# Kernel optimization log

Hardware: AMD Instinct MI355X
Metric: run time of the kernel (lower is better)

Reference implementation:

```python
import jax, jax.numpy as jnp
import numpy as np

_SAMPLING_EPS = 1e-5
_NEG_INF = -jnp.inf


def _apply_min_p(logits, min_p):
    # probs >= min_p * max_prob are kept (vLLM apply_min_p)
    probs = jax.nn.softmax(logits, axis=-1)
    max_p = jnp.max(probs, axis=-1, keepdims=True)
    keep = probs >= (min_p[:, None] * max_p)
    return jnp.where(keep, logits, _NEG_INF)


def _apply_top_k_top_p(logits, top_k, top_p):
    # One descending sort serves both filters (mirrors vLLM topk/topp kernel).
    T, V = logits.shape
    sorted_l = jnp.sort(logits, axis=-1)[:, ::-1]  # [T, V] descending
    # top-k threshold: k-th largest logit; top_k <= 0 means disabled
    k = jnp.where(top_k <= 0, V, jnp.clip(top_k, 1, V)).astype(jnp.int32)
    kth = jnp.take_along_axis(sorted_l, (k - 1)[:, None], axis=-1)  # [T, 1]
    # top-p: keep smallest prefix whose prob mass reaches top_p (first token always kept)
    probs = jax.nn.softmax(sorted_l, axis=-1)
    cum = jnp.cumsum(probs, axis=-1)
    keep_p = (cum - probs) < top_p[:, None]
    pth = jnp.min(jnp.where(keep_p, sorted_l, jnp.inf), axis=-1, keepdims=True)
    keep = (logits >= kth) & (logits >= pth)
    return jnp.where(keep, logits, _NEG_INF)


def _gather_logprobs(logprobs, num_logprobs, token_ids):
    # vLLM gather_logprobs: topk + sampled-token logprob + rank
    topk_lp, topk_idx = jax.lax.top_k(logprobs, num_logprobs)  # [T, K]
    tok = token_ids[:, None]  # [T, 1]
    tok_lp = jnp.take_along_axis(logprobs, tok, axis=-1)  # [T, 1]
    ranks = jnp.sum(logprobs >= tok_lp, axis=-1).astype(jnp.int32)  # [T]
    indices = jnp.concatenate([tok, topk_idx], axis=1).astype(jnp.int32)
    lps = jnp.concatenate([tok_lp, topk_lp], axis=1)
    return indices, lps, ranks


def setup_inputs() -> dict:
    key = jax.random.key(0)
    k1, k2, k3, k4, k5, k6 = jax.random.split(key, 6)
    T, V = 256, 128256
    logits = jax.random.normal(k1, (T, V), dtype=jnp.float32)
    temperature = 0.2 + 1.3 * jax.random.uniform(k2, (T,), dtype=jnp.float32)
    # every 8th request is greedy (temperature < _SAMPLING_EPS path)
    temperature = jnp.where(jnp.arange(T) % 8 == 0, 0.0, temperature)
    min_p = 0.05 * jax.random.uniform(k3, (T,), dtype=jnp.float32)
    top_p = 0.5 + 0.5 * jax.random.uniform(k4, (T,), dtype=jnp.float32)
    top_k = jax.random.randint(k5, (T,), 0, 64, dtype=jnp.int32)
    u = jax.random.uniform(k6, (T, V), dtype=jnp.float32, minval=1e-10, maxval=1.0)
    return {"logits": logits, "temperature": temperature, "min_p": min_p,
            "top_p": top_p, "top_k": top_k, "u": u, "num_logprobs": 20}


def reference(logits, temperature, min_p, top_p, top_k, u, num_logprobs):
    logits = logits.astype(jnp.float32)
    # logprobs computed on raw (pre-temperature) logits, as in vLLM
    raw_logprobs = jax.nn.log_softmax(logits, axis=-1)
    # greedy path
    greedy = jnp.argmax(logits, axis=-1)
    # random path: temperature -> min_p -> top-k/top-p -> gumbel-max sample
    is_greedy = temperature < _SAMPLING_EPS
    safe_temp = jnp.where(is_greedy, 1.0, temperature)  # rows with temp<eps use greedy anyway
    l = logits / safe_temp[:, None]
    l = _apply_min_p(l, min_p)
    l = _apply_top_k_top_p(l, top_k, top_p)
    gumbel = -jnp.log(-jnp.log(u))  # u in (0,1)
    random_sampled = jnp.argmax(l + gumbel, axis=-1)
    sampled = jnp.where(is_greedy, greedy, random_sampled)
    indices, lps, ranks = _gather_logprobs(raw_logprobs, num_logprobs, sampled)
    sampled_token_ids = sampled.astype(jnp.int32)[:, None]  # [T, 1]
    return sampled_token_ids, indices, lps, ranks
```

## Files before the change

### kernel.cpp

```cpp
#include <hip/hip_runtime.h>
#include <math.h>

#define TPB 1024
#define TPBS 256
#define NS 8
#define NBINS 512
#define CAP 2048
#define NSEL 64
#define MBINS 1024
#define MWIN 16.0f
#define WIN 2.0f
#define SLCAP 1024
#define BANDCAP 64

typedef unsigned long long u64t;

__device__ __forceinline__ unsigned int ordAsc(float v) {
  unsigned int b = __float_as_uint(v);
  return (b & 0x80000000u) ? ~b : (b | 0x80000000u);
}
__device__ __forceinline__ float ordInv(unsigned int o) {
  return __uint_as_float((o & 0x80000000u) ? (o & 0x7fffffffu) : ~o);
}
__device__ __forceinline__ unsigned int fkeyDesc(float v) { return ~ordAsc(v); }
__device__ __forceinline__ float fkeyInv(unsigned int kd) { return ordInv(~kd); }
__device__ __forceinline__ u64t mkMaxKey(float v, int idx) {
  return ((u64t)ordAsc(v) << 32) | (unsigned int)(~(unsigned int)idx);
}

__device__ __forceinline__ float blockSumF(float v, float* sred) {
  #pragma unroll
  for (int o = 32; o > 0; o >>= 1) v += __shfl_down(v, o, 64);
  int wid = threadIdx.x >> 6, lane = threadIdx.x & 63, nw = blockDim.x >> 6;
  __syncthreads();
  if (lane == 0) sred[wid] = v;
  __syncthreads();
  if (threadIdx.x == 0) { float r = sred[0]; for (int w = 1; w < nw; ++w) r += sred[w]; sred[0] = r; }
  __syncthreads();
  float r = sred[0];
  __syncthreads();
  return r;
}
__device__ __forceinline__ int blockSumI(int v, int* sred) {
  #pragma unroll
  for (int o = 32; o > 0; o >>= 1) v += __shfl_down(v, o, 64);
  int wid = threadIdx.x >> 6, lane = threadIdx.x & 63, nw = blockDim.x >> 6;
  __syncthreads();
  if (lane == 0) sred[wid] = v;
  __syncthreads();
  if (threadIdx.x == 0) { int r = sred[0]; for (int w = 1; w < nw; ++w) r += sred[w]; sred[0] = r; }
  __syncthreads();
  int r = sred[0];
  __syncthreads();
  return r;
}
__device__ __forceinline__ int blockMaxI(int v, int* sred) {
  #pragma unroll
  for (int o = 32; o > 0; o >>= 1) { int v2 = __shfl_down(v, o, 64); if (v2 > v) v = v2; }
  int wid = threadIdx.x >> 6, lane = threadIdx.x & 63, nw = blockDim.x >> 6;
  __syncthreads();
  if (lane == 0) sred[wid] = v;
  __syncthreads();
  if (threadIdx.x == 0) { int r = sred[0]; for (int w = 1; w < nw; ++w) if (sred[w] > r) r = sred[w]; sred[0] = r; }
  __syncthreads();
  int r = sred[0];
  __syncthreads();
  return r;
}
__device__ __forceinline__ u64t blockMaxU64(u64t v, u64t* sred) {
  #pragma unroll
  for (int o = 32; o > 0; o >>= 1) { u64t v2 = __shfl_down(v, o, 64); if (v2 > v) v = v2; }
  int wid = threadIdx.x >> 6, lane = threadIdx.x & 63, nw = blockDim.x >> 6;
  __syncthreads();
  if (lane == 0) sred[wid] = v;
  __syncthreads();
  if (threadIdx.x == 0) { u64t r = sred[0]; for (int w = 1; w < nw; ++w) if (sred[w] > r) r = sred[w]; sred[0] = r; }
  __syncthreads();
  u64t r = sred[0];
  __syncthreads();
  return r;
}
__device__ __forceinline__ void blockArgMaxF(float& v, int& idx, float* sredf, int* sredi) {
  #pragma unroll
  for (int o = 32; o > 0; o >>= 1) {
    float v2 = __shfl_down(v, o, 64);
    int  i2 = __shfl_down(idx, o, 64);
    if (v2 > v || (v2 == v && i2 < idx)) { v = v2; idx = i2; }
  }
  int wid = threadIdx.x >> 6, lane = threadIdx.x & 63, nw = blockDim.x >> 6;
  __syncthreads();
  if (lane == 0) { sredf[wid] = v; sredi[wid] = idx; }
  __syncthreads();
  if (threadIdx.x == 0) {
    float bv = sredf[0]; int bi = sredi[0];
    for (int w = 1; w < nw; ++w) {
      float v2 = sredf[w]; int i2 = sredi[w];
      if (v2 > bv || (v2 == bv && i2 < bi)) { bv = v2; bi = i2; }
    }
    sredf[0] = bv; sredi[0] = bi;
  }
  __syncthreads();
  v = sredf[0]; idx = sredi[0];
  __syncthreads();
}

__device__ void bitonicSortN(u64t* keys, int n) {
  for (unsigned int k = 2; k <= (unsigned int)n; k <<= 1) {
    for (unsigned int j = k >> 1; j > 0; j >>= 1) {
      __syncthreads();
      for (unsigned int i = threadIdx.x; i < (unsigned int)n; i += blockDim.x) {
        unsigned int ixj = i ^ j;
        if (ixj > i) {
          u64t a = keys[i], b = keys[ixj];
          bool up = ((i & k) == 0);
          if ((a > b) == up) { keys[i] = b; keys[ixj] = a; }
        }
      }
    }
  }
  __syncthreads();
}

__device__ u64t bitonicReg1024(u64t key, u64t* lds) {
  const int tid = threadIdx.x;
  for (unsigned int k = 2; k <= 1024; k <<= 1) {
    for (unsigned int j = k >> 1; j > 0; j >>= 1) {
      u64t partner;
      if (j >= 64) {
        __syncthreads();
        lds[tid] = key;
        __syncthreads();
        partner = lds[tid ^ j];
      } else {
        partner = __shfl_xor((unsigned long long)key, (int)j, 64);
      }
      bool up = ((tid & k) == 0);
      bool lower = ((tid & j) == 0);
      bool keepSmaller = (up == lower);
      bool pSmaller = (partner < key);
      if (keepSmaller == pSmaller) key = partner;
    }
  }
  __syncthreads();
  lds[tid] = key;
  __syncthreads();
  return key;
}

__device__ __forceinline__ float combineS0(const u64t* smax, const float* s0s, float m0) {
  float S0 = 0.f;
  for (int w = 0; w < NS; ++w) {
    float ms = ordInv((unsigned int)(smax[w] >> 32));
    S0 += s0s[w] * expf(ms - m0);
  }
  return S0;
}

__global__ __launch_bounds__(TPBS) void k1_max(const float* __restrict__ logits,
                                               u64t* __restrict__ maxes,
                                               float* __restrict__ s0_ws,
                                               int* __restrict__ ccnt,
                                               int* __restrict__ bandcnt, int V) {
  const int row = blockIdx.y, s = blockIdx.x, tid = threadIdx.x;
  if (s == 0 && tid == 0) { ccnt[row] = 0; bandcnt[row] = 0; }
  const float* x = logits + (size_t)row * V;
  const int V4 = V >> 2;
  const float4* x4 = (const float4*)x;
  const int a4 = (int)(((long long)V4 * s) / NS), b4 = (int)(((long long)V4 * (s + 1)) / NS);
  u64t best = 0ull;
  for (int i4 = a4 + tid; i4 < b4; i4 += TPBS) {
    float4 v = x4[i4]; int b = i4 << 2;
    u64t k0 = mkMaxKey(v.x, b);     if (k0 > best) best = k0;
    u64t k1 = mkMaxKey(v.y, b + 1); if (k1 > best) best = k1;
    u64t k2 = mkMaxKey(v.z, b + 2); if (k2 > best) best = k2;
    u64t k3 = mkMaxKey(v.w, b + 3); if (k3 > best) best = k3;
  }
  if (s == NS - 1) for (int i = (V4 << 2) + tid; i < V; i += TPBS) {
    u64t k = mkMaxKey(x[i], i); if (k > best) best = k;
  }
  __shared__ u64t sredU[16];
  __shared__ float sredF[16];
  best = blockMaxU64(best, sredU);
  if (tid == 0) maxes[row * NS + s] = best;
  const float msv = ordInv((unsigned int)(best >> 32));
  float s0 = 0.f;
  for (int i4 = a4 + tid; i4 < b4; i4 += TPBS) {
    float4 v = x4[i4];
    s0 += expf(v.x - msv) + expf(v.y - msv) + expf(v.z - msv) + expf(v.w - msv);
  }
  if (s == NS - 1) for (int i = (V4 << 2) + tid; i < V; i += TPBS) s0 += expf(x[i] - msv);
  float r0 = blockSumF(s0, sredF);
  if (tid == 0) s0_ws[row * NS + s] = r0;
}

__global__ __launch_bounds__(TPBS) void k2_all(const float* __restrict__ logits,
    const float* __restrict__ temp_arr, const float* __restrict__ minp_arr,
    const int* __restrict__ topk_arr, const u64t* __restrict__ maxes,
    float* __restrict__ sl_ws, float* __restrict__ sp_ws, int* __restrict__ ck_ws,
    int* __restrict__ ccnt, u64t* __restrict__ cand,
    int* __restrict__ bandcnt, u64t* __restrict__ band,
    u64t* __restrict__ mass, int V) {
  const int row = blockIdx.y, s = blockIdx.x, tid = threadIdx.x;
  __shared__ u64t smax[NS];
  __shared__ float sredF[16];
  __shared__ int sredI[16];
  __shared__ u64t lcand[SLCAP];
  __shared__ u64t lmass[MBINS];
  __shared__ int lcnt, lbase;
  const float temp = temp_arr[row];
  const bool greedy = (temp < 1e-5f);
  const int topk = topk_arr[row];
  const bool deep = (!greedy && topk <= 0);
  if (tid < NS) smax[tid] = maxes[row * NS + tid];
  if (tid == 0) lcnt = 0;
  if (deep) for (int b = tid; b < MBINS; b += TPBS) lmass[b] = 0ull;
  __syncthreads();
  u64t mk = smax[0];
  for (int w = 1; w < NS; ++w) { u64t t = smax[w]; if (t > mk) mk = t; }
  const float m0 = ordInv((unsigned int)(mk >> 32));
  const float wlo = m0 - WIN;
  const float* x = logits + (size_t)row * V;
  const int V4 = V >> 2;
  const float4* x4 = (const float4*)x;
  const int a4 = (int)(((long long)V4 * s) / NS), b4 = (int)(((long long)V4 * (s + 1)) / NS);

  if (greedy) {
    auto bodyG = [&](float vv, int gi) {
      if (vv >= wlo) {
        int pos = atomicAdd(&lcnt, 1);
        if (pos < SLCAP) lcand[pos] = ((u64t)fkeyDesc(vv) << 32) | (unsigned int)gi;
      }
    };
    for (int i4 = a4 + tid; i4 < b4; i4 += TPBS) {
      float4 v = x4[i4]; int b = i4 << 2;
      bodyG(v.x, b); bodyG(v.y, b + 1); bodyG(v.z, b + 2); bodyG(v.w, b + 3);
    }
    if (s == NS - 1) for (int i = (V4 << 2) + tid; i < V; i += TPBS) bodyG(x[i], i);
    __syncthreads();
    if (tid == 0) {
      sl_ws[row * NS + s] = 0.f; sp_ws[row * NS + s] = 0.f; ck_ws[row * NS + s] = 0;
      int c = lcnt;
      int add = (c > SLCAP) ? (c + CAP + 1) : c;
      lbase = atomicAdd(&ccnt[row], add);
    }
    __syncthreads();
    int c = lcnt < SLCAP ? lcnt : SLCAP;
    int base = lbase;
    for (int j = tid; j < c; j += TPBS) {
      int pos = base + j;
      if (pos < CAP) cand[(size_t)row * CAP + pos] = lcand[j];
    }
    return;
  }

  const float st = temp;
  const float ml = m0 / st;
  const float minp = minp_arr[row];
  const float bHi = minp * (1.0f + 4e-6f);
  const float bLo = minp * (1.0f - 4e-6f);
  const float scaleM = (float)MBINS / MWIN;
  float sl = 0.f, sp = 0.f; int ckp = 0;
  auto body = [&](float vv, int gi) {
    float l = vv / st;
    float e = expf(l - ml);
    sl += e;
    if (minp <= 0.f || e > bHi) {
      sp += e; ckp++;
      if (deep) {
        float fm = (m0 - vv) * scaleM;
        if (fm < (float)MBINS)
          atomicAdd(&lmass[(int)fm], (u64t)((double)e * 4294967296.0));
      }
    } else if (e >= bLo) {
      int pos = atomicAdd(&bandcnt[row], 1);
      if (pos < BANDCAP)
        band[(size_t)row * BANDCAP + pos] = ((u64t)(unsigned int)gi << 32) | __float_as_uint(vv);
    }
    if (vv >= wlo) {
      int pos = atomicAdd(&lcnt, 1);
      if (pos < SLCAP) lcand[pos] = ((u64t)fkeyDesc(vv) << 32) | (unsigned int)gi;
    }
  };
  for (int i4 = a4 + tid; i4 < b4; i4 += TPBS) {
    float4 v = x4[i4]; int b = i4 << 2;
    body(v.x, b); body(v.y, b + 1); body(v.z, b + 2); body(v.w, b + 3);
  }
  if (s == NS - 1) for (int i = (V4 << 2) + tid; i < V; i += TPBS) body(x[i], i);
  float rl = blockSumF(sl, sredF);
  float rp = blockSumF(sp, sredF);
  int rc = blockSumI(ckp, sredI);
  if (tid == 0) {
    sl_ws[row * NS + s] = rl; sp_ws[row * NS + s] = rp; ck_ws[row * NS + s] = rc;
    int c = lcnt;
    int add = (c > SLCAP) ? (c + CAP + 1) : c;
    lbase = atomicAdd(&ccnt[row], add);
  }
  __syncthreads();
  int c = lcnt < SLCAP ? lcnt : SLCAP;
  int base = lbase;
  for (int j = tid; j < c; j += TPBS) {
    int pos = base + j;
    if (pos < CAP) cand[(size_t)row * CAP + pos] = lcand[j];
  }
  if (deep) {
    u64t* mrow = mass + ((size_t)row * NS + s) * MBINS;
    for (int b = tid; b < MBINS; b += TPBS) mrow[b] = lmass[b];
  }
}

__global__ __launch_bounds__(TPB) void k5_final(const float* __restrict__ logits,
    const float* __restrict__ temp_arr, const float* __restrict__ minp_arr,
    const float* __restrict__ topp_arr, const int* __restrict__ topk_arr,
    const float* __restrict__ u_arr, const u64t* __restrict__ maxes,
    const float* __restrict__ s0_ws, const float* __restrict__ sl_ws,
    const float* __restrict__ sp_ws, const int* __restrict__ ck_ws,
    const int* __restrict__ ccnt, const u64t* __restrict__ cand,
    const u64t* __restrict__ mass, const u64t* __restrict__ band,
    const int* __restrict__ bandcnt, float* __restrict__ w_thr,
    int* __restrict__ w_bpM, double* __restrict__ w_seed, float* __restrict__ w_spD,
    float* __restrict__ out, int T, int V, int NL) {
  __shared__ u64t keyA[CAP];
  __shared__ int fh[NBINS];
  __shared__ float sredF[16];
  __shared__ int sredI[16];
  __shared__ u64t smax[NS];
  __shared__ float sp0[NS], spl[NS], spsp[NS];
  __shared__ int spck[NS];
  __shared__ float sh_thresh, sh_toklp, sh_spAdd;
  __shared__ double sh_seed;
  __shared__ int sh_cnt, sh_bp, sh_bCnt, sh_ckAdd;
  __shared__ u64t sh_bKeys[BANDCAP];
  __shared__ u64t sh_bMass[BANDCAP];
  __shared__ int  sh_bBin[BANDCAP];
  __shared__ u64t kb64[NSEL];
  __shared__ u64t kbs[NSEL];

  const int row = blockIdx.x;
  const int tid = threadIdx.x;
  const float* x  = logits + (size_t)row * V;
  const float* uu = u_arr  + (size_t)row * V;
  const float temp = temp_arr[row];
  const float minp = minp_arr[row];
  const float topp = topp_arr[row];
  const int   topk = topk_arr[row];
  const bool greedy = (temp < 1e-5f);
  const float st = greedy ? 1.0f : temp;
  const int V4 = V >> 2;
  const float4* x4 = (const float4*)x;

  if (tid < NS) {
    smax[tid] = maxes[row * NS + tid];
    sp0[tid] = s0_ws[row * NS + tid];
    spl[tid] = sl_ws[row * NS + tid];
    spsp[tid] = sp_ws[row * NS + tid];
    spck[tid] = ck_ws[row * NS + tid];
  }
  __syncthreads();
  u64t mk = smax[0];
  for (int w = 1; w < NS; ++w) { u64t t = smax[w]; if (t > mk) mk = t; }
  const float m0 = ordInv((unsigned int)(mk >> 32));
  const int gidx = (int)(~(unsigned int)mk);
  float S = spl[0], Sp = spsp[0];
  int ck = spck[0];
  for (int w = 1; w < NS; ++w) { S += spl[w]; Sp += spsp[w]; ck += spck[w]; }
  const float S0 = combineS0(smax, sp0, m0);
  const float ml = m0 / st;
  const float logS0 = logf(S0);
  const float rhs = minp * (1.0f / S);
  const float rhsS = rhs * S;
  const float rhsHi = rhsS * (1.0f + 1e-6f);
  const float rhsLo = rhsS * (1.0f - 1e-6f);
  auto keepTest = [&](float e) -> bool {
    if (e > rhsHi) return true;
    if (e < rhsLo) return false;
    return (e / S) >= rhs;
  };
  const bool deep = (!greedy && topk <= 0);
  const float scaleM = (float)MBINS / MWIN;

  const int bandTotal = greedy ? 0 : bandcnt[row];
  const bool bandOv = bandTotal > BANDCAP;
  if (tid == 0) { sh_bCnt = 0; sh_spAdd = 0.f; sh_ckAdd = 0; }
  __syncthreads();
  if (!greedy && !bandOv && bandTotal > 0 && minp > 0.f) {
    if (tid == 0) {
      for (int i = 0; i < bandTotal; ++i) sh_bKeys[i] = band[(size_t)row * BANDCAP + i];
      for (int i = 1; i < bandTotal; ++i) {
        u64t k = sh_bKeys[i]; int j = i - 1;
        while (j >= 0 && sh_bKeys[j] > k) { sh_bKeys[j + 1] = sh_bKeys[j]; j--; }
        sh_bKeys[j + 1] = k;
      }
      float spAdd = 0.f; int ckAdd = 0, bc = 0;
      for (int i = 0; i < bandTotal; ++i) {
        float vv = __uint_as_float((unsigned int)(sh_bKeys[i] & 0xffffffffu));
        float l = vv / st; float e = expf(l - ml);
        if ((e / S) >= rhs) {
          spAdd += e; ckAdd++;
          if (deep) {
            float fm = (m0 - vv) * scaleM;
            if (fm < (float)MBINS) { sh_bBin[bc] = (int)fm; sh_bMass[bc] = (u64t)((double)e * 4294967296.0); bc++; }
          }
        }
      }
      sh_spAdd = spAdd; sh_ckAdd = ckAdd; sh_bCnt = bc;
    }
    __syncthreads();
    Sp += sh_spAdd; ck += sh_ckAdd;
  } else if (!greedy && bandOv) {
    float sp2 = 0.f; int ck2 = 0;
    auto bodyR = [&](float vv) {
      float l = vv / st; float e = expf(l - ml);
      if (keepTest(e)) { sp2 += e; ck2++; }
    };
    for (int i4 = tid; i4 < V4; i4 += TPB) { float4 v = x4[i4]; bodyR(v.x); bodyR(v.y); bodyR(v.z); bodyR(v.w); }
    for (int i = (V4 << 2) + tid; i < V; i += TPB) bodyR(x[i]);
    Sp = blockSumF(sp2, sredF);
    ck = blockSumI(ck2, sredI);
  }

  int cc = ccnt[row];
  int Cact = cc < CAP ? cc : CAP;
  int need = NSEL;
  if (topk > need) need = topk;
  if (need > CAP / 2) need = CAP / 2;
  if (need > V) need = V;
  bool fb = (cc > CAP) || (Cact < need);
  if (!fb) {
    for (int j = tid; j < Cact; j += TPB) keyA[j] = cand[(size_t)row * CAP + j];
  } else {
    const float bS = (float)NBINS / MWIN;
    for (int b = tid; b < NBINS; b += TPB) fh[b] = 0;
    if (tid == 0) sh_cnt = 0;
    __syncthreads();
    auto hb = [&](float vv) {
      float fbv = (m0 - vv) * bS;
      if (fbv < (float)NBINS) atomicAdd(&fh[(int)fbv], 1);
    };
    for (int i4 = tid; i4 < V4; i4 += TPB) { float4 v = x4[i4]; hb(v.x); hb(v.y); hb(v.z); hb(v.w); }
    for (int i = (V4 << 2) + tid; i < V; i += TPB) hb(x[i]);
    __syncthreads();
    if (tid == 0) {
      int cum = 0, B = -1;
      for (int b = 0; b < NBINS; ++b) { cum += fh[b]; if (cum >= need) { B = b; break; } }
      if (B < 0) B = NBINS - 1;
      sh_bp = B;
    }
    __syncthreads();
    const int B = sh_bp;
    auto cb = [&](float vv, int gi) {
      float fbv = (m0 - vv) * bS;
      if (fbv < (float)NBINS && (int)fbv <= B) {
        int pos = atomicAdd(&sh_cnt, 1);
        if (pos < CAP) keyA[pos] = ((u64t)fkeyDesc(vv) << 32) | (unsigned int)gi;
      }
    };
    for (int i4 = tid; i4 < V4; i4 += TPB) { float4 v = x4[i4]; int b = i4 << 2; cb(v.x, b); cb(v.y, b + 1); cb(v.z, b + 2); cb(v.w, b + 3); }
    for (int i = (V4 << 2) + tid; i < V; i += TPB) cb(x[i], i);
    __syncthreads();
    Cact = sh_cnt < CAP ? sh_cnt : CAP;
  }
  __syncthreads();
  if (Cact <= 1024) {
    u64t ka = (tid < Cact) ? keyA[tid] : ~0ull;
    bitonicReg1024(ka, keyA);
  } else {
    int n = 128; while (n < Cact) n <<= 1;
    for (int i = Cact + tid; i < n; i += TPB) keyA[i] = ~0ull;
    __syncthreads();
    bitonicSortN(keyA, n);
  }
  {
    int M = Cact < NSEL ? Cact : NSEL;
    if (tid < M) {
      u64t ka = keyA[tid];
      float xv = fkeyInv((unsigned int)(ka >> 32));
      float lp = (xv - m0) - logS0;
      kb64[tid] = ((u64t)fkeyDesc(lp) << 32) | (ka & 0xffffffffu);
    }
    __syncthreads();
    if (tid < M) {
      u64t me = kb64[tid];
      int r = 0;
      for (int i = 0; i < M; ++i) r += (kb64[i] < me) ? 1 : 0;
      kbs[r] = me;
    }
    __syncthreads();
    float* o_idx  = out + T;
    float* o_lps  = out + T + (size_t)T * (NL + 1);
    for (int j = tid; j < NL; j += TPB) {
      if (j < M) {
        u64t kb = kbs[j];
        o_idx[(size_t)row * (NL + 1) + 1 + j] = (float)(unsigned int)(kb & 0xffffffffu);
        o_lps[(size_t)row * (NL + 1) + 1 + j] = fkeyInv((unsigned int)(kb >> 32));
      }
    }
  }

  int sampled = -1;
  if (greedy) {
    sampled = gidx;
  } else if (topk > 0) {
    if (tid == 0) {
      int k = topk; if (k > V) k = V; if (k > CAP) k = CAP;
      int jp = 0; float cum = 0.f;
      for (int j = 0; j < k; ++j) {
        float pj = 0.f;
        if (j < ck && j < Cact) {
          float xv = fkeyInv((unsigned int)(keyA[j] >> 32));
          pj = expf(xv / st - ml) / Sp;
        }
        cum += pj;
        float ex = cum - pj;
        if (ex < topp) jp = j;
      }
      float thr;
      if (jp < ck && jp < Cact) {
        float xv = fkeyInv((unsigned int)(keyA[jp] >> 32));
        thr = xv / st;
      } else thr = -INFINITY;
      sh_thresh = thr;
    }
    __syncthreads();
    const float thr = sh_thresh;
    float bm = -INFINITY; int bi = 0x7fffffff;
    for (int j = tid; j < Cact; j += TPB) {
      u64t ka = keyA[j];
      float xv = fkeyInv((unsigned int)(ka >> 32));
      int gi = (int)(ka & 0xffffffffu);
      float l = xv / st;
      float e = expf(l - ml);
      if (keepTest(e) && l >= thr) {
        float uv = uu[gi];
        float g = -logf(-logf(uv));
        float val = l + g;
        if (val > bm || (val == bm && gi < bi)) { bm = val; bi = gi; }
      }
    }
    blockArgMaxF(bm, bi, sredF, sredI);
    sampled = bi;
  } else {
    if (!bandOv) {
      if (tid < MBINS) {
        u64t m = 0;
        for (int w = 0; w < NS; ++w) m += mass[((size_t)row * NS + w) * MBINS + tid];
        int bc = sh_bCnt;
        for (int j = 0; j < bc; ++j) if (sh_bBin[j] == tid) m += sh_bMass[j];
        keyA[tid] = m;
      }
    } else {
      for (int b = tid; b < MBINS; b += TPB) keyA[b] = 0ull;
      __syncthreads();
      auto bodyM = [&](float vv) {
        float l = vv / st; float e = expf(l - ml);
        if (keepTest(e)) {
          float fm = (m0 - vv) * scaleM;
          if (fm < (float)MBINS) atomicAdd(&keyA[(int)fm], (u64t)((double)e * 4294967296.0));
        }
      };
      for (int i4 = tid; i4 < V4; i4 += TPB) { float4 v = x4[i4]; bodyM(v.x); bodyM(v.y); bodyM(v.z); bodyM(v.w); }
      for (int i = (V4 << 2) + tid; i < V; i += TPB) bodyM(x[i]);
    }
    __syncthreads();
    u64t mh = (tid < MBINS) ? keyA[tid] : 0ull;
    for (int off = 1; off < MBINS; off <<= 1) {
      u64t add = (tid < MBINS && tid >= off) ? keyA[tid - off] : 0ull;
      __syncthreads();
      if (tid < MBINS) keyA[tid] += add;
      __syncthreads();
    }
    const double TP = (double)topp * (double)Sp;
    int q = -1; u64t myexcl = 0;
    if (tid < MBINS && mh > 0ull) {
      u64t excl = keyA[tid] - mh;
      if ((double)excl * (1.0 / 4294967296.0) < TP) { q = tid; myexcl = excl; }
    }
    int bp = blockMaxI(q, sredI);
    if (bp >= 0 && tid == bp) sh_seed = (double)myexcl * (1.0 / 4294967296.0);
    if (bp < 0 && tid == 0) sh_seed = 0.0;
    __syncthreads();
    if (tid == 0) {
      w_bpM[row] = bp;
      w_seed[row] = sh_seed;
      w_spD[row] = Sp;
      if (bp < 0) w_thr[row] = -INFINITY;
    }
  }

  if (!deep) {
    if (tid == 0) sh_toklp = (x[sampled] - m0) - logS0;
    __syncthreads();
    const float toklp = sh_toklp;
    int rc = 0;
    for (int j = tid; j < Cact; j += TPB) {
      float xv = fkeyInv((unsigned int)(keyA[j] >> 32));
      float lp = (xv - m0) - logS0;
      if (lp >= toklp) rc++;
    }
    int rank = blockSumI(rc, sredI);
    float* o_samp = out;
    float* o_idx  = out + T;
    float* o_lps  = out + T + (size_t)T * (NL + 1);
    float* o_rank = out + T + (size_t)2 * T * (NL + 1);
    if (tid == 0) {
      o_samp[row] = (float)sampled;
      o_idx[(size_t)row * (NL + 1)] = (float)sampled;
      o_lps[(size_t)row * (NL + 1)] = toklp;
      o_rank[row] = (float)rank;
    }
  }
}

__global__ __launch_bounds__(TPB) void kD_thr(const float* __restrict__ logits,
    const float* __restrict__ temp_arr, const float* __restrict__ minp_arr,
    const float* __restrict__ topp_arr, const int* __restrict__ topk_arr,
    const u64t* __restrict__ maxes, const float* __restrict__ sl_ws,
    const int* __restrict__ w_bpM, const float* __restrict__ w_spD,
    const double* __restrict__ w_seed, float* __restrict__ w_thr, int V) {
  const int row = blockIdx.x, tid = threadIdx.x;
  const float temp = temp_arr[row];
  if (temp < 1e-5f || topk_arr[row] > 0) return;
  const int bp = w_bpM[row];
  if (bp < 0) return;
  __shared__ u64t keyA[CAP];
  __shared__ float pvals[CAP];
  __shared__ u64t smax[NS];
  __shared__ float ssl[NS];
  __shared__ int sh_cnt;
  if (tid < NS) { smax[tid] = maxes[row * NS + tid]; ssl[tid] = sl_ws[row * NS + tid]; }
  if (tid == 0) sh_cnt = 0;
  __syncthreads();
  u64t mk = smax[0];
  for (int w = 1; w < NS; ++w) { u64t t = smax[w]; if (t > mk) mk = t; }
  float S = ssl[0];
  for (int w = 1; w < NS; ++w) S += ssl[w];
  const float m0 = ordInv((unsigned int)(mk >> 32));
  const float st = temp;
  const float ml = m0 / st;
  const float minp = minp_arr[row];
  const float rhs = minp * (1.0f / S);
  const float rhsS = rhs * S;
  const float rhsHi = rhsS * (1.0f + 1e-6f);
  const float rhsLo = rhsS * (1.0f - 1e-6f);
  auto keepTest = [&](float e) -> bool {
    if (e > rhsHi) return true;
    if (e < rhsLo) return false;
    return (e / S) >= rhs;
  };
  const float scaleM = (float)MBINS / MWIN;
  const float* x = logits + (size_t)row * V;
  const int V4 = V >> 2;
  const float4* x4 = (const float4*)x;
  auto body = [&](float vv, int gi) {
    float fm = (m0 - vv) * scaleM;
    if (fm < (float)MBINS && (int)fm == bp) {
      float l = vv / st;
      float e = expf(l - ml);
      if (keepTest(e)) {
        int pos = atomicAdd(&sh_cnt, 1);
        if (pos < CAP) keyA[pos] = ((u64t)fkeyDesc(vv) << 32) | (unsigned int)gi;
      }
    }
  };
  for (int i4 = tid; i4 < V4; i4 += TPB) {
    float4 v = x4[i4]; int b = i4 << 2;
    body(v.x, b); body(v.y, b + 1); body(v.z, b + 2); body(v.w, b + 3);
  }
  for (int i = (V4 << 2) + tid; i < V; i += TPB) body(x[i], i);
  __syncthreads();
  int C5 = sh_cnt < CAP ? sh_cnt : CAP;
  if (C5 <= 1024) {
    u64t kc = (tid < C5) ? keyA[tid] : ~0ull;
    bitonicReg1024(kc, keyA);
  } else {
    int n5 = 128; while (n5 < C5) n5 <<= 1;
    for (int i = C5 + tid; i < n5; i += TPB) keyA[i] = ~0ull;
    __syncthreads();
    bitonicSortN(keyA, n5);
  }
  const float Sp = w_spD[row];
  for (int j = tid; j < C5; j += TPB) {
    float xv = fkeyInv((unsigned int)(keyA[j] >> 32));
    pvals[j] = expf(xv / st - ml) / Sp;
  }
  __syncthreads();
  if (tid == 0) {
    const float topp = topp_arr[row];
    float cum = (float)(w_seed[row] / (double)Sp);
    float lastVal = fkeyInv((unsigned int)(keyA[0] >> 32));
    for (int j = 0; j < C5; ++j) {
      float pj = pvals[j];
      cum += pj;
      float ex = cum - pj;
      if (ex < topp) lastVal = fkeyInv((unsigned int)(keyA[j] >> 32));
    }
    w_thr[row] = lastVal / st;
  }
}

__global__ __launch_bounds__(TPBS) void k6_gumbel(const float* __restrict__ logits,
    const float* __restrict__ temp_arr, const float* __restrict__ minp_arr,
    const int* __restrict__ topk_arr, const float* __restrict__ u_arr,
    const u64t* __restrict__ maxes, const float* __restrict__ sl_ws,
    const float* __restrict__ w_thr, u64t* __restrict__ gkey, int V) {
  const int row = blockIdx.y, s = blockIdx.x, tid = threadIdx.x;
  const float temp = temp_arr[row];
  if (temp < 1e-5f || topk_arr[row] > 0) return;
  __shared__ u64t smax[NS];
  __shared__ float ssl[NS];
  __shared__ float sredF[16];
  __shared__ int sredI[16];
  if (tid < NS) { smax[tid] = maxes[row * NS + tid]; ssl[tid] = sl_ws[row * NS + tid]; }
  __syncthreads();
  u64t mk = smax[0];
  for (int w = 1; w < NS; ++w) { u64t t = smax[w]; if (t > mk) mk = t; }
  float S = ssl[0];
  for (int w = 1; w < NS; ++w) S += ssl[w];
  const float m0 = ordInv((unsigned int)(mk >> 32));
  const float st = temp;
  const float ml = m0 / st;
  const float minp = minp_arr[row];
  const float rhs = minp * (1.0f / S);
  const float rhsS = rhs * S;
  const float rhsHi = rhsS * (1.0f + 1e-6f);
  const float rhsLo = rhsS * (1.0f - 1e-6f);
  auto keepTest = [&](float e) -> bool {
    if (e > rhsHi) return true;
    if (e < rhsLo) return false;
    return (e / S) >= rhs;
  };
  const float thr = w_thr[row];
  const float* x  = logits + (size_t)row * V;
  const float* uu = u_arr  + (size_t)row * V;
  const int V4 = V >> 2;
  const float4* x4 = (const float4*)x;
  const float4* u4 = (const float4*)uu;
  const int a4 = (int)(((long long)V4 * s) / NS), b4 = (int)(((long long)V4 * (s + 1)) / NS);
  float bm = -INFINITY; int bi = 0x7fffffff;
  auto body = [&](float vv, float uv, int gi) {
    float l = vv / st;
    float e = expf(l - ml);
    if (keepTest(e) && l >= thr) {
      float g = -logf(-logf(uv));
      float val = l + g;
      if (val > bm || (val == bm && gi < bi)) { bm = val; bi = gi; }
    }
  };
  for (int i4 = a4 + tid; i4 < b4; i4 += TPBS) {
    float4 v = x4[i4]; float4 w = u4[i4]; int b = i4 << 2;
    body(v.x, w.x, b); body(v.y, w.y, b + 1); body(v.z, w.z, b + 2); body(v.w, w.w, b + 3);
  }
  if (s == NS - 1) for (int i = (V4 << 2) + tid; i < V; i += TPBS) body(x[i], uu[i], i);
  blockArgMaxF(bm, bi, sredF, sredI);
  if (tid == 0) gkey[row * NS + s] = mkMaxKey(bm, bi);
}

__global__ __launch_bounds__(TPB) void k7_deepfin(const float* __restrict__ logits,
    const float* __restrict__ temp_arr, const int* __restrict__ topk_arr,
    const u64t* __restrict__ gkey, const float* __restrict__ s0_ws,
    const u64t* __restrict__ maxes, float* __restrict__ out, int T, int V, int NL) {
  const int row = blockIdx.x, tid = threadIdx.x;
  const float temp = temp_arr[row];
  if (temp < 1e-5f || topk_arr[row] > 0) return;
  __shared__ u64t sg[NS];
  __shared__ u64t smax[NS];
  __shared__ float sp0[NS];
  __shared__ int sredI[16];
  if (tid < NS) { sg[tid] = gkey[row * NS + tid]; smax[tid] = maxes[row * NS + tid]; sp0[tid] = s0_ws[row * NS + tid]; }
  __syncthreads();
  u64t gk = sg[0];
  for (int w = 1; w < NS; ++w) { if (sg[w] > gk) gk = sg[w]; }
  u64t mk = smax[0];
  for (int w = 1; w < NS; ++w) { u64t t = smax[w]; if (t > mk) mk = t; }
  const float m0 = ordInv((unsigned int)(mk >> 32));
  const float S0 = combineS0(smax, sp0, m0);
  const float logS0 = logf(S0);
  const int sampled = (int)(~(unsigned int)gk);
  const float* x = logits + (size_t)row * V;
  const float toklp = (x[sampled] - m0) - logS0;
  const int V4 = V >> 2;
  const float4* x4 = (const float4*)x;
  int rc = 0;
  auto body = [&](float vv) {
    float lp = (vv - m0) - logS0;
    if (lp >= toklp) rc++;
  };
  for (int i4 = tid; i4 < V4; i4 += TPB) { float4 v = x4[i4]; body(v.x); body(v.y); body(v.z); body(v.w); }
  for (int i = (V4 << 2) + tid; i < V; i += TPB) body(x[i]);
  int rank = blockSumI(rc, sredI);
  float* o_samp = out;
  float* o_idx  = out + T;
  float* o_lps  = out + T + (size_t)T * (NL + 1);
  float* o_rank = out + T + (size_t)2 * T * (NL + 1);
  if (tid == 0) {
    o_samp[row] = (float)sampled;
    o_idx[(size_t)row * (NL + 1)] = (float)sampled;
    o_lps[(size_t)row * (NL + 1)] = toklp;
    o_rank[row] = (float)rank;
  }
}

__global__ __launch_bounds__(TPB) void sampler_mono(
    const float* __restrict__ logits, const float* __restrict__ temp_arr,
    const float* __restrict__ minp_arr, const float* __restrict__ topp_arr,
    const int* __restrict__ topk_arr, const float* __restrict__ u_arr,
    float* __restrict__ out, int T, int V, int NL) {
  __shared__ u64t keyA[CAP];
  __shared__ u64t keyB[CAP];
  __shared__ float pvals[CAP];
  __shared__ int   cnthist[NBINS];
  __shared__ u64t  masshist[NBINS];
  __shared__ float sredF[16];
  __shared__ int   sredI[16];
  __shared__ float sh_thresh, sh_toklp, sh_Rm, sh_Roff;
  __shared__ double sh_seedD, sh_seedBase;
  __shared__ int sh_B64, sh_Bp, sh_cnt, sh_state;

  const int row = blockIdx.x;
  const int tid = threadIdx.x;
  const float* x  = logits + (size_t)row * V;
  const float* uu = u_arr  + (size_t)row * V;
  const float temp = temp_arr[row];
  const float minp = minp_arr[row];
  const float topp = topp_arr[row];
  const int   topk = topk_arr[row];
  const bool greedy = (temp < 1e-5f);
  const float st = greedy ? 1.0f : temp;
  const int V4 = V >> 2;
  const float4* x4 = (const float4*)x;

  float m0; int gidx;
  {
    float lm = -INFINITY; int lidx = 0x7fffffff;
    for (int i4 = tid; i4 < V4; i4 += TPB) {
      float4 v = x4[i4]; int b = i4 << 2;
      if (v.x > lm) { lm = v.x; lidx = b; }
      if (v.y > lm) { lm = v.y; lidx = b + 1; }
      if (v.z > lm) { lm = v.z; lidx = b + 2; }
      if (v.w > lm) { lm = v.w; lidx = b + 3; }
    }
    for (int i = (V4 << 2) + tid; i < V; i += TPB) {
      float v = x[i]; if (v > lm) { lm = v; lidx = i; }
    }
    blockArgMaxF(lm, lidx, sredF, sredI);
    m0 = lm; gidx = lidx;
  }
  const float ml = m0 / st;

  float Rcur = 2.0f;
  float binScale = (float)NBINS / Rcur;
  for (int b = tid; b < NBINS; b += TPB) cnthist[b] = 0;
  __syncthreads();
  float S0, S;
  {
    float s0p = 0.f, slp = 0.f;
    auto histAdd = [&](float vv) {
      float fb = (m0 - vv) * binScale;
      if (fb < (float)NBINS) atomicAdd(&cnthist[(int)fb], 1);
    };
    for (int i4 = tid; i4 < V4; i4 += TPB) {
      float4 v = x4[i4];
      s0p += expf(v.x - m0) + expf(v.y - m0) + expf(v.z - m0) + expf(v.w - m0);
      if (!greedy) slp += expf(v.x / st - ml) + expf(v.y / st - ml) + expf(v.z / st - ml) + expf(v.w / st - ml);
      histAdd(v.x); histAdd(v.y); histAdd(v.z); histAdd(v.w);
    }
    for (int i = (V4 << 2) + tid; i < V; i += TPB) {
      float v = x[i]; s0p += expf(v - m0); if (!greedy) slp += expf(v / st - ml); histAdd(v);
    }
    S0 = blockSumF(s0p, sredF);
    S = greedy ? S0 : blockSumF(slp, sredF);
  }

  int need = NSEL;
  if (topk > need) need = topk;
  if (need > CAP / 2) need = CAP / 2;
  if (need > V) need = V;
  int B64;
  for (int attempt = 0; ; ++attempt) {
    __syncthreads();
    if (tid == 0) {
      long long cum = 0; int b64 = -1; long long c64 = 0;
      for (int b = 0; b < NBINS; ++b) {
        cum += cnthist[b];
        if (cum >= need) { b64 = b; c64 = cum; break; }
      }
      int state;
      if (b64 >= 0 && c64 <= CAP) state = 1;
      else if (b64 < 0) state = 0;
      else state = 2;
      if (attempt >= 3 && state != 1) { state = 1; if (b64 < 0) b64 = NBINS - 1; }
      sh_state = state; sh_B64 = b64;
    }
    __syncthreads();
    if (sh_state == 1) { B64 = sh_B64; break; }
    Rcur = (sh_state == 0) ? Rcur * 8.0f : Rcur * 0.125f;
    binScale = (float)NBINS / Rcur;
    __syncthreads();
    for (int b = tid; b < NBINS; b += TPB) cnthist[b] = 0;
    __syncthreads();
    auto histAdd2 = [&](float vv) {
      float fb = (m0 - vv) * binScale;
      if (fb < (float)NBINS) atomicAdd(&cnthist[(int)fb], 1);
    };
    for (int i4 = tid; i4 < V4; i4 += TPB) {
      float4 v = x4[i4];
      histAdd2(v.x); histAdd2(v.y); histAdd2(v.z); histAdd2(v.w);
    }
    for (int i = (V4 << 2) + tid; i < V; i += TPB) histAdd2(x[i]);
  }

  const float logS0 = logf(S0);
  const float rhs = minp * (1.0f / S);
  const float rhsS = rhs * S;
  const float rhsHi = rhsS * (1.0f + 1e-6f);
  const float rhsLo = rhsS * (1.0f - 1e-6f);
  auto keepTest = [&](float e) -> bool {
    if (e > rhsHi) return true;
    if (e < rhsLo) return false;
    return (e / S) >= rhs;
  };
  const bool needMass = (!greedy && topk <= 0);
  const float scaleM0 = (float)NBINS / 16.0f;

  for (int b = tid; b < NBINS; b += TPB) { cnthist[b] = 0; masshist[b] = 0ull; }
  if (tid == 0) { sh_cnt = 0; sh_Rm = 16.0f; sh_Roff = 0.0f; sh_seedBase = 0.0; }
  __syncthreads();
  float Sp; int ck;
  {
    float spp = 0.f; int ckp = 0;
    auto bodyB = [&](float vv, int gi) {
      float fb = (m0 - vv) * binScale;
      if (fb < (float)NBINS && (int)fb <= B64) {
        int pos = atomicAdd(&sh_cnt, 1);
        if (pos < CAP) keyA[pos] = ((u64t)fkeyDesc(vv) << 32) | (unsigned int)gi;
      }
      if (!greedy) {
        float l = vv / st;
        float e = expf(l - ml);
        if (keepTest(e)) {
          spp += e; ckp++;
          if (needMass) {
            float fm = (m0 - vv) * scaleM0;
            if (fm < (float)NBINS) {
              int bm = (int)fm;
              atomicAdd(&masshist[bm], (u64t)((double)e * 4294967296.0));
              atomicAdd(&cnthist[bm], 1);
            }
          }
        }
      }
    };
    for (int i4 = tid; i4 < V4; i4 += TPB) {
      float4 v = x4[i4]; int b = i4 << 2;
      bodyB(v.x, b); bodyB(v.y, b + 1); bodyB(v.z, b + 2); bodyB(v.w, b + 3);
    }
    for (int i = (V4 << 2) + tid; i < V; i += TPB) bodyB(x[i], i);
    Sp = blockSumF(spp, sredF);
    ck = blockSumI(ckp, sredI);
  }
  int Cact = sh_cnt; if (Cact > CAP) Cact = CAP;

  int n = 128; while (n < Cact) n <<= 1;
  for (int i = Cact + tid; i < n; i += TPB) keyA[i] = ~0ull;
  __syncthreads();
  bitonicSortN(keyA, n);
  for (int j = tid; j < n; j += TPB) {
    if (j < Cact) {
      u64t ka = keyA[j];
      float xv = fkeyInv((unsigned int)(ka >> 32));
      float lp = (xv - m0) - logS0;
      keyB[j] = ((u64t)fkeyDesc(lp) << 32) | (ka & 0xffffffffu);
    } else keyB[j] = ~0ull;
  }
  bitonicSortN(keyB, n);

  int sampled;
  if (greedy) {
    sampled = gidx;
  } else if (topk > 0) {
    if (tid == 0) {
      int k = topk; if (k > V) k = V; if (k > CAP) k = CAP;
      int jp = 0; float cum = 0.f;
      for (int j = 0; j < k; ++j) {
        float pj = 0.f;
        if (j < ck && j < Cact) {
          float xv = fkeyInv((unsigned int)(keyA[j] >> 32));
          pj = expf(xv / st - ml) / Sp;
        }
        cum += pj;
        float ex = cum - pj;
        if (ex < topp) jp = j;
      }
      float thr;
      if (jp < ck && jp < Cact) {
        float xv = fkeyInv((unsigned int)(keyA[jp] >> 32));
        thr = xv / st;
      } else thr = -INFINITY;
      sh_thresh = thr;
    }
    __syncthreads();
    const float thr = sh_thresh;
    float bm = -INFINITY; int bi = 0x7fffffff;
    for (int j = tid; j < Cact; j += TPB) {
      u64t ka = keyA[j];
      float xv = fkeyInv((unsigned int)(ka >> 32));
      int gi = (int)(ka & 0xffffffffu);
      float l = xv / st;
      float e = expf(l - ml);
      if (keepTest(e) && l >= thr) {
        float uv = uu[gi];
        float g = -logf(-logf(uv));
        float val = l + g;
        if (val > bm || (val == bm && gi < bi)) { bm = val; bi = gi; }
      }
    }
    blockArgMaxF(bm, bi, sredF, sredI);
    sampled = bi;
  } else {
    for (int attempt = 0; ; ++attempt) {
      __syncthreads();
      if (tid == 0) {
        float Rm = sh_Rm, Roff = sh_Roff;
        double TP = (double)topp * (double)Sp;
        double cm = sh_seedBase; int bp = -1; double seed = sh_seedBase; int cbp = 0;
        for (int b = 0; b < NBINS; ++b) {
          u64t mh = masshist[b];
          if (mh > 0ull && cm < TP) { bp = b; seed = cm; cbp = cnthist[b]; }
          cm += (double)mh * (1.0 / 4294967296.0);
        }
        int state = 1;
        if (attempt < 3) {
          if (cm < TP && Roff == 0.0f) {
            state = 0; sh_Rm = Rm * 8.0f;
          } else if (bp >= 0 && cbp > CAP) {
            state = 2;
            float bw = Rm / (float)NBINS;
            sh_Roff = Roff + (float)bp * bw;
            sh_Rm = bw;
            sh_seedBase = seed;
          }
        }
        if (bp < 0) { bp = 0; seed = sh_seedBase; }
        sh_Bp = bp; sh_seedD = seed; sh_state = state;
      }
      __syncthreads();
      if (sh_state == 1) break;
      float Rm = sh_Rm, Roff = sh_Roff;
      float sM = (float)NBINS / Rm;
      for (int b = tid; b < NBINS; b += TPB) { cnthist[b] = 0; masshist[b] = 0ull; }
      __syncthreads();
      auto bodyM = [&](float vv) {
        float fm = ((m0 - vv) - Roff) * sM;
        if (fm >= 0.f && fm < (float)NBINS) {
          float l = vv / st;
          float e = expf(l - ml);
          if (keepTest(e)) {
            int bm = (int)fm;
            atomicAdd(&masshist[bm], (u64t)((double)e * 4294967296.0));
            atomicAdd(&cnthist[bm], 1);
          }
        }
      };
      for (int i4 = tid; i4 < V4; i4 += TPB) {
        float4 v = x4[i4]; bodyM(v.x); bodyM(v.y); bodyM(v.z); bodyM(v.w);
      }
      for (int i = (V4 << 2) + tid; i < V; i += TPB) bodyM(x[i]);
    }
    const int Bp = sh_Bp;
    const float RmF = sh_Rm, RoffF = sh_Roff;
    const float sM = (float)NBINS / RmF;
    if (tid == 0) sh_cnt = 0;
    __syncthreads();
    auto bodyC = [&](float vv, int gi) {
      float fm = ((m0 - vv) - RoffF) * sM;
      if (fm >= 0.f && fm < (float)NBINS && (int)fm == Bp) {
        float l = vv / st;
        float e = expf(l - ml);
        if (keepTest(e)) {
          int pos = atomicAdd(&sh_cnt, 1);
          if (pos < CAP) keyA[pos] = ((u64t)fkeyDesc(vv) << 32) | (unsigned int)gi;
        }
      }
    };
    for (int i4 = tid; i4 < V4; i4 += TPB) {
      float4 v = x4[i4]; int b = i4 << 2;
      bodyC(v.x, b); bodyC(v.y, b + 1); bodyC(v.z, b + 2); bodyC(v.w, b + 3);
    }
    for (int i = (V4 << 2) + tid; i < V; i += TPB) bodyC(x[i], i);
    __syncthreads();
    int C5 = sh_cnt; if (C5 > CAP) C5 = CAP;
    int n5 = 128; while (n5 < C5) n5 <<= 1;
    for (int i = C5 + tid; i < n5; i += TPB) keyA[i] = ~0ull;
    __syncthreads();
    bitonicSortN(keyA, n5);
    for (int j = tid; j < C5; j += TPB) {
      float xv = fkeyInv((unsigned int)(keyA[j] >> 32));
      pvals[j] = expf(xv / st - ml) / Sp;
    }
    __syncthreads();
    if (tid == 0) {
      float cum = (float)(sh_seedD / (double)Sp);
      float lastVal = fkeyInv((unsigned int)(keyA[0] >> 32));
      for (int j = 0; j < C5; ++j) {
        float pj = pvals[j];
        cum += pj;
        float ex = cum - pj;
        if (ex < topp) lastVal = fkeyInv((unsigned int)(keyA[j] >> 32));
      }
      sh_thresh = lastVal / st;
    }
    __syncthreads();
    const float thr = sh_thresh;
    const float4* u4 = (const float4*)uu;
    float bm = -INFINITY; int bi = 0x7fffffff;
    auto body6 = [&](float vv, float uv, int gi) {
      float l = vv / st;
      float e = expf(l - ml);
      if (keepTest(e) && l >= thr) {
        float g = -logf(-logf(uv));
        float val = l + g;
        if (val > bm || (val == bm && gi < bi)) { bm = val; bi = gi; }
      }
    };
    for (int i4 = tid; i4 < V4; i4 += TPB) {
      float4 v = x4[i4]; float4 w = u4[i4]; int b = i4 << 2;
      body6(v.x, w.x, b); body6(v.y, w.y, b + 1); body6(v.z, w.z, b + 2); body6(v.w, w.w, b + 3);
    }
    for (int i = (V4 << 2) + tid; i < V; i += TPB) body6(x[i], uu[i], i);
    blockArgMaxF(bm, bi, sredF, sredI);
    sampled = bi;
  }

  if (tid == 0) sh_toklp = (x[sampled] - m0) - logS0;
  __syncthreads();
  const float toklp = sh_toklp;
  int rank;
  {
    int rc = 0;
    if (!needMass) {
      for (int j = tid; j < Cact; j += TPB) {
        float xv = fkeyInv((unsigned int)(keyA[j] >> 32));
        float lp = (xv - m0) - logS0;
        if (lp >= toklp) rc++;
      }
    } else {
      auto body7 = [&](float vv) {
        float lp = (vv - m0) - logS0;
        if (lp >= toklp) rc++;
      };
      for (int i4 = tid; i4 < V4; i4 += TPB) {
        float4 v = x4[i4]; body7(v.x); body7(v.y); body7(v.z); body7(v.w);
      }
      for (int i = (V4 << 2) + tid; i < V; i += TPB) body7(x[i]);
    }
    rank = blockSumI(rc, sredI);
  }

  float* o_samp = out;
  float* o_idx  = out + T;
  float* o_lps  = out + T + (size_t)T * (NL + 1);
  float* o_rank = out + T + (size_t)2 * T * (NL + 1);
  if (tid == 0) {
    o_samp[row] = (float)sampled;
    o_idx[(size_t)row * (NL + 1)] = (float)sampled;
    o_lps[(size_t)row * (NL + 1)] = toklp;
    o_rank[row] = (float)rank;
  }
  for (int j = tid; j < NL; j += TPB) {
    u64t kb = keyB[j];
    o_idx[(size_t)row * (NL + 1) + 1 + j] = (float)(unsigned int)(kb & 0xffffffffu);
    o_lps[(size_t)row * (NL + 1) + 1 + j] = fkeyInv((unsigned int)(kb >> 32));
  }
}

extern "C" void kernel_launch(void* const* d_in, const int* in_sizes, int n_in,
                              void* d_out, int out_size, void* d_ws, size_t ws_size,
                              hipStream_t stream) {
  const float* logits = (const float*)d_in[0];
  const float* temp   = (const float*)d_in[1];
  const float* minp   = (const float*)d_in[2];
  const float* topp   = (const float*)d_in[3];
  const int*   topk   = (const int*)d_in[4];
  const float* u      = (const float*)d_in[5];
  const int T  = in_sizes[1];
  const int V  = in_sizes[0] / T;
  const int NL = (out_size / T - 4) / 2;

  size_t off = 0;
  char* base = (char*)d_ws;
  u64t*   w_maxes   = (u64t*)(base + off);   off += (size_t)T * NS * 8;
  u64t*   w_cand    = (u64t*)(base + off);   off += (size_t)T * CAP * 8;
  u64t*   w_mass    = (u64t*)(base + off);   off += (size_t)T * NS * MBINS * 8;
  u64t*   w_gkey    = (u64t*)(base + off);   off += (size_t)T * NS * 8;
  u64t*   w_band    = (u64t*)(base + off);   off += (size_t)T * BANDCAP * 8;
  double* w_seed    = (double*)(base + off); off += (size_t)T * 8;
  float*  w_s0      = (float*)(base + off);  off += (size_t)T * NS * 4;
  float*  w_sl      = (float*)(base + off);  off += (size_t)T * NS * 4;
  float*  w_sp      = (float*)(base + off);  off += (size_t)T * NS * 4;
  int*    w_ck      = (int*)(base + off);    off += (size_t)T * NS * 4;
  int*    w_ccnt    = (int*)(base + off);    off += (size_t)T * 4;
  int*    w_bandcnt = (int*)(base + off);    off += (size_t)T * 4;
  float*  w_thr     = (float*)(base + off);  off += (size_t)T * 4;
  int*    w_bpM     = (int*)(base + off);    off += (size_t)T * 4;
  float*  w_spD     = (float*)(base + off);  off += (size_t)T * 4;

  if (off > ws_size) {
    sampler_mono<<<T, TPB, 0, stream>>>(logits, temp, minp, topp, topk, u,
                                        (float*)d_out, T, V, NL);
    return;
  }

  dim3 gS(NS, T);
  k1_max<<<gS, TPBS, 0, stream>>>(logits, w_maxes, w_s0, w_ccnt, w_bandcnt, V);
  k2_all<<<gS, TPBS, 0, stream>>>(logits, temp, minp, topk, w_maxes, w_sl,
                                  w_sp, w_ck, w_ccnt, w_cand, w_bandcnt, w_band,
                                  w_mass, V);
  k5_final<<<T, TPB, 0, stream>>>(logits, temp, minp, topp, topk, u, w_maxes,
                                  w_s0, w_sl, w_sp, w_ck, w_ccnt, w_cand, w_mass,
                                  w_band, w_bandcnt, w_thr, w_bpM, w_seed, w_spD,
                                  (float*)d_out, T, V, NL);
  kD_thr<<<T, TPB, 0, stream>>>(logits, temp, minp, topp, topk, w_maxes, w_sl,
                                w_bpM, w_spD, w_seed, w_thr, V);
  k6_gumbel<<<gS, TPBS, 0, stream>>>(logits, temp, minp, topk, u, w_maxes, w_sl,
                                     w_thr, w_gkey, V);
  k7_deepfin<<<T, TPB, 0, stream>>>(logits, temp, topk, w_gkey, w_s0, w_maxes,
                                    (float*)d_out, T, V, NL);
}
```

Baseline: 212.7 us.

## Fuse sampler pipeline into one kernel with per-row inter-block spin barriers

Replaces the six-kernel chain (max, stats, final, threshold, gumbel, deep-finish) with a single fused kernel plus a small zeroing kernel. Each row is now handled by 4 cooperating blocks instead of 8, and they synchronise through global atomic counters used as row-level barriers. The separate exp-sum pass from the old max kernel is folded into the stats pass using the global row max. This targets launch gaps and repeated reads of the logits. The cost is that the grid relies on all blocks of a row being resident at once for the spin barriers to finish, and each row now gets less parallelism.

```diff
diff --git a/kernel.cpp b/kernel.cpp
--- a/kernel.cpp
+++ b/kernel.cpp
@@ -1,10 +1,12 @@
 #include <hip/hip_runtime.h>
 #include <math.h>
 
+#define TPBS 256
 #define TPB 1024
-#define TPBS 256
-#define NS 8
+#define NS 4
+#define NBAR 8
 #define NBINS 512
+#define FBBINS 256
 #define CAP 2048
 #define NSEL 64
 #define MBINS 1024
@@ -121,222 +123,52 @@
   __syncthreads();
 }
 
-__device__ u64t bitonicReg1024(u64t key, u64t* lds) {
-  const int tid = threadIdx.x;
-  for (unsigned int k = 2; k <= 1024; k <<= 1) {
-    for (unsigned int j = k >> 1; j > 0; j >>= 1) {
-      u64t partner;
-      if (j >= 64) {
-        __syncthreads();
-        lds[tid] = key;
-        __syncthreads();
-        partner = lds[tid ^ j];
-      } else {
-        partner = __shfl_xor((unsigned long long)key, (int)j, 64);
-      }
-      bool up = ((tid & k) == 0);
-      bool lower = ((tid & j) == 0);
-      bool keepSmaller = (up == lower);
-      bool pSmaller = (partner < key);
-      if (keepSmaller == pSmaller) key = partner;
-    }
-  }
-  __syncthreads();
-  lds[tid] = key;
-  __syncthreads();
-  return key;
-}
-
-__device__ __forceinline__ float combineS0(const u64t* smax, const float* s0s, float m0) {
-  float S0 = 0.f;
-  for (int w = 0; w < NS; ++w) {
-    float ms = ordInv((unsigned int)(smax[w] >> 32));
-    S0 += s0s[w] * expf(ms - m0);
-  }
-  return S0;
-}
-
-__global__ __launch_bounds__(TPBS) void k1_max(const float* __restrict__ logits,
-                                               u64t* __restrict__ maxes,
-                                               float* __restrict__ s0_ws,
-                                               int* __restrict__ ccnt,
-                                               int* __restrict__ bandcnt, int V) {
-  const int row = blockIdx.y, s = blockIdx.x, tid = threadIdx.x;
-  if (s == 0 && tid == 0) { ccnt[row] = 0; bandcnt[row] = 0; }
-  const float* x = logits + (size_t)row * V;
-  const int V4 = V >> 2;
-  const float4* x4 = (const float4*)x;
-  const int a4 = (int)(((long long)V4 * s) / NS), b4 = (int)(((long long)V4 * (s + 1)) / NS);
-  u64t best = 0ull;
-  for (int i4 = a4 + tid; i4 < b4; i4 += TPBS) {
-    float4 v = x4[i4]; int b = i4 << 2;
-    u64t k0 = mkMaxKey(v.x, b);     if (k0 > best) best = k0;
-    u64t k1 = mkMaxKey(v.y, b + 1); if (k1 > best) best = k1;
-    u64t k2 = mkMaxKey(v.z, b + 2); if (k2 > best) best = k2;
-    u64t k3 = mkMaxKey(v.w, b + 3); if (k3 > best) best = k3;
-  }
-  if (s == NS - 1) for (int i = (V4 << 2) + tid; i < V; i += TPBS) {
-    u64t k = mkMaxKey(x[i], i); if (k > best) best = k;
-  }
-  __shared__ u64t sredU[16];
-  __shared__ float sredF[16];
-  best = blockMaxU64(best, sredU);
-  if (tid == 0) maxes[row * NS + s] = best;
-  const float msv = ordInv((unsigned int)(best >> 32));
-  float s0 = 0.f;
-  for (int i4 = a4 + tid; i4 < b4; i4 += TPBS) {
-    float4 v = x4[i4];
-    s0 += expf(v.x - msv) + expf(v.y - msv) + expf(v.z - msv) + expf(v.w - msv);
-  }
-  if (s == NS - 1) for (int i = (V4 << 2) + tid; i < V; i += TPBS) s0 += expf(x[i] - msv);
-  float r0 = blockSumF(s0, sredF);
-  if (tid == 0) s0_ws[row * NS + s] = r0;
-}
-
-__global__ __launch_bounds__(TPBS) void k2_all(const float* __restrict__ logits,
-    const float* __restrict__ temp_arr, const float* __restrict__ minp_arr,
-    const int* __restrict__ topk_arr, const u64t* __restrict__ maxes,
-    float* __restrict__ sl_ws, float* __restrict__ sp_ws, int* __restrict__ ck_ws,
-    int* __restrict__ ccnt, u64t* __restrict__ cand,
-    int* __restrict__ bandcnt, u64t* __restrict__ band,
-    u64t* __restrict__ mass, int V) {
-  const int row = blockIdx.y, s = blockIdx.x, tid = threadIdx.x;
+__device__ __forceinline__ void rowBarrier(int* ctr) {
+  __syncthreads();
+  __threadfence();
+  if (threadIdx.x == 0) {
+    atomicAdd(ctr, 1);
+    while (__hip_atomic_load(ctr, __ATOMIC_ACQUIRE, __HIP_MEMORY_SCOPE_AGENT) < NS)
+      __builtin_amdgcn_s_sleep(2);
+  }
+  __syncthreads();
+  __threadfence();
+}
+
+__global__ void k0_zero(int* __restrict__ p, int n) {
+  int i = blockIdx.x * blockDim.x + threadIdx.x;
+  if (i < n) p[i] = 0;
+}
+
+__global__ __launch_bounds__(TPBS, 6) void fused(
+    const float* __restrict__ logits, const float* __restrict__ temp_arr,
+    const float* __restrict__ minp_arr, const float* __restrict__ topp_arr,
+    const int* __restrict__ topk_arr, const float* __restrict__ u_arr,
+    u64t* __restrict__ maxes, u64t* __restrict__ cand, u64t* __restrict__ mass,
+    u64t* __restrict__ gkey, u64t* __restrict__ band,
+    float* __restrict__ s0_ws, float* __restrict__ sl_ws, float* __restrict__ sp_ws,
+    int* __restrict__ ck_ws, int* __restrict__ ccnt, int* __restrict__ bandcnt,
+    int* __restrict__ ccnt2, int* __restrict__ rankAcc,
+    float* __restrict__ w_thr, int* __restrict__ w_bp,
+    int* __restrict__ w_sampled, float* __restrict__ w_toklp,
+    int* __restrict__ bars, float* __restrict__ out, int T, int V, int NL) {
+  __shared__ u64t bufA[CAP];
   __shared__ u64t smax[NS];
+  __shared__ float s0s[NS], sls[NS], sps[NS];
+  __shared__ int scks[NS];
   __shared__ float sredF[16];
   __shared__ int sredI[16];
-  __shared__ u64t lcand[SLCAP];
-  __shared__ u64t lmass[MBINS];
-  __shared__ int lcnt, lbase;
-  const float temp = temp_arr[row];
-  const bool greedy = (temp < 1e-5f);
-  const int topk = topk_arr[row];
-  const bool deep = (!greedy && topk <= 0);
-  if (tid < NS) smax[tid] = maxes[row * NS + tid];
-  if (tid == 0) lcnt = 0;
-  if (deep) for (int b = tid; b < MBINS; b += TPBS) lmass[b] = 0ull;
-  __syncthreads();
-  u64t mk = smax[0];
-  for (int w = 1; w < NS; ++w) { u64t t = smax[w]; if (t > mk) mk = t; }
-  const float m0 = ordInv((unsigned int)(mk >> 32));
-  const float wlo = m0 - WIN;
-  const float* x = logits + (size_t)row * V;
-  const int V4 = V >> 2;
-  const float4* x4 = (const float4*)x;
-  const int a4 = (int)(((long long)V4 * s) / NS), b4 = (int)(((long long)V4 * (s + 1)) / NS);
-
-  if (greedy) {
-    auto bodyG = [&](float vv, int gi) {
-      if (vv >= wlo) {
-        int pos = atomicAdd(&lcnt, 1);
-        if (pos < SLCAP) lcand[pos] = ((u64t)fkeyDesc(vv) << 32) | (unsigned int)gi;
-      }
-    };
-    for (int i4 = a4 + tid; i4 < b4; i4 += TPBS) {
-      float4 v = x4[i4]; int b = i4 << 2;
-      bodyG(v.x, b); bodyG(v.y, b + 1); bodyG(v.z, b + 2); bodyG(v.w, b + 3);
-    }
-    if (s == NS - 1) for (int i = (V4 << 2) + tid; i < V; i += TPBS) bodyG(x[i], i);
-    __syncthreads();
-    if (tid == 0) {
-      sl_ws[row * NS + s] = 0.f; sp_ws[row * NS + s] = 0.f; ck_ws[row * NS + s] = 0;
-      int c = lcnt;
-      int add = (c > SLCAP) ? (c + CAP + 1) : c;
-      lbase = atomicAdd(&ccnt[row], add);
-    }
-    __syncthreads();
-    int c = lcnt < SLCAP ? lcnt : SLCAP;
-    int base = lbase;
-    for (int j = tid; j < c; j += TPBS) {
-      int pos = base + j;
-      if (pos < CAP) cand[(size_t)row * CAP + pos] = lcand[j];
-    }
-    return;
-  }
-
-  const float st = temp;
-  const float ml = m0 / st;
-  const float minp = minp_arr[row];
-  const float bHi = minp * (1.0f + 4e-6f);
-  const float bLo = minp * (1.0f - 4e-6f);
-  const float scaleM = (float)MBINS / MWIN;
-  float sl = 0.f, sp = 0.f; int ckp = 0;
-  auto body = [&](float vv, int gi) {
-    float l = vv / st;
-    float e = expf(l - ml);
-    sl += e;
-    if (minp <= 0.f || e > bHi) {
-      sp += e; ckp++;
-      if (deep) {
-        float fm = (m0 - vv) * scaleM;
-        if (fm < (float)MBINS)
-          atomicAdd(&lmass[(int)fm], (u64t)((double)e * 4294967296.0));
-      }
-    } else if (e >= bLo) {
-      int pos = atomicAdd(&bandcnt[row], 1);
-      if (pos < BANDCAP)
-        band[(size_t)row * BANDCAP + pos] = ((u64t)(unsigned int)gi << 32) | __float_as_uint(vv);
-    }
-    if (vv >= wlo) {
-      int pos = atomicAdd(&lcnt, 1);
-      if (pos < SLCAP) lcand[pos] = ((u64t)fkeyDesc(vv) << 32) | (unsigned int)gi;
-    }
-  };
-  for (int i4 = a4 + tid; i4 < b4; i4 += TPBS) {
-    float4 v = x4[i4]; int b = i4 << 2;
-    body(v.x, b); body(v.y, b + 1); body(v.z, b + 2); body(v.w, b + 3);
-  }
-  if (s == NS - 1) for (int i = (V4 << 2) + tid; i < V; i += TPBS) body(x[i], i);
-  float rl = blockSumF(sl, sredF);
-  float rp = blockSumF(sp, sredF);
-  int rc = blockSumI(ckp, sredI);
-  if (tid == 0) {
-    sl_ws[row * NS + s] = rl; sp_ws[row * NS + s] = rp; ck_ws[row * NS + s] = rc;
-    int c = lcnt;
-    int add = (c > SLCAP) ? (c + CAP + 1) : c;
-    lbase = atomicAdd(&ccnt[row], add);
-  }
-  __syncthreads();
-  int c = lcnt < SLCAP ? lcnt : SLCAP;
-  int base = lbase;
-  for (int j = tid; j < c; j += TPBS) {
-    int pos = base + j;
-    if (pos < CAP) cand[(size_t)row * CAP + pos] = lcand[j];
-  }
-  if (deep) {
-    u64t* mrow = mass + ((size_t)row * NS + s) * MBINS;
-    for (int b = tid; b < MBINS; b += TPBS) mrow[b] = lmass[b];
-  }
-}
-
-__global__ __launch_bounds__(TPB) void k5_final(const float* __restrict__ logits,
-    const float* __restrict__ temp_arr, const float* __restrict__ minp_arr,
-    const float* __restrict__ topp_arr, const int* __restrict__ topk_arr,
-    const float* __restrict__ u_arr, const u64t* __restrict__ maxes,
-    const float* __restrict__ s0_ws, const float* __restrict__ sl_ws,
-    const float* __restrict__ sp_ws, const int* __restrict__ ck_ws,
-    const int* __restrict__ ccnt, const u64t* __restrict__ cand,
-    const u64t* __restrict__ mass, const u64t* __restrict__ band,
-    const int* __restrict__ bandcnt, float* __restrict__ w_thr,
-    int* __restrict__ w_bpM, double* __restrict__ w_seed, float* __restrict__ w_spD,
-    float* __restrict__ out, int T, int V, int NL) {
-  __shared__ u64t keyA[CAP];
-  __shared__ int fh[NBINS];
-  __shared__ float sredF[16];
-  __shared__ int sredI[16];
-  __shared__ u64t smax[NS];
-  __shared__ float sp0[NS], spl[NS], spsp[NS];
-  __shared__ int spck[NS];
-  __shared__ float sh_thresh, sh_toklp, sh_spAdd;
-  __shared__ double sh_seed;
-  __shared__ int sh_cnt, sh_bp, sh_bCnt, sh_ckAdd;
+  __shared__ u64t sredU[16];
   __shared__ u64t sh_bKeys[BANDCAP];
   __shared__ u64t sh_bMass[BANDCAP];
   __shared__ int  sh_bBin[BANDCAP];
-  __shared__ u64t kb64[NSEL];
-  __shared__ u64t kbs[NSEL];
-
-  const int row = blockIdx.x;
-  const int tid = threadIdx.x;
+  __shared__ u64t kbuf[2 * NSEL];
+  __shared__ int lcnt, lbase, sh_cnt, sh_bCnt, sh_ckAdd;
+  __shared__ float sh_thresh, sh_spAdd;
+  __shared__ double sh_seedD;
+
+  const int s = blockIdx.x, row = blockIdx.y, tid = threadIdx.x;
+  int* myBar = bars + row * NBAR;
   const float* x  = logits + (size_t)row * V;
   const float* uu = u_arr  + (size_t)row * V;
   const float temp = temp_arr[row];
@@ -344,458 +176,522 @@
   const float topp = topp_arr[row];
   const int   topk = topk_arr[row];
   const bool greedy = (temp < 1e-5f);
+  const bool deep = (!greedy && topk <= 0);
   const float st = greedy ? 1.0f : temp;
   const int V4 = V >> 2;
   const float4* x4 = (const float4*)x;
-
-  if (tid < NS) {
-    smax[tid] = maxes[row * NS + tid];
-    sp0[tid] = s0_ws[row * NS + tid];
-    spl[tid] = sl_ws[row * NS + tid];
-    spsp[tid] = sp_ws[row * NS + tid];
-    spck[tid] = ck_ws[row * NS + tid];
-  }
+  const int a4 = (int)(((long long)V4 * s) / NS), b4 = (int)(((long long)V4 * (s + 1)) / NS);
+
+  {
+    u64t best = 0ull;
+    for (int i4 = a4 + tid; i4 < b4; i4 += TPBS) {
+      float4 v = x4[i4]; int b = i4 << 2;
+      u64t k0 = mkMaxKey(v.x, b);     if (k0 > best) best = k0;
+      u64t k1 = mkMaxKey(v.y, b + 1); if (k1 > best) best = k1;
+      u64t k2 = mkMaxKey(v.z, b + 2); if (k2 > best) best = k2;
+      u64t k3 = mkMaxKey(v.w, b + 3); if (k3 > best) best = k3;
+    }
+    if (s == NS - 1) for (int i = (V4 << 2) + tid; i < V; i += TPBS) {
+      u64t k = mkMaxKey(x[i], i); if (k > best) best = k;
+    }
+    best = blockMaxU64(best, sredU);
+    if (tid == 0) maxes[row * NS + s] = best;
+  }
+  rowBarrier(&myBar[0]);
+
+  if (tid < NS) smax[tid] = maxes[row * NS + tid];
+  if (tid == 0) lcnt = 0;
   __syncthreads();
   u64t mk = smax[0];
   for (int w = 1; w < NS; ++w) { u64t t = smax[w]; if (t > mk) mk = t; }
   const float m0 = ordInv((unsigned int)(mk >> 32));
   const int gidx = (int)(~(unsigned int)mk);
-  float S = spl[0], Sp = spsp[0];
-  int ck = spck[0];
-  for (int w = 1; w < NS; ++w) { S += spl[w]; Sp += spsp[w]; ck += spck[w]; }
-  const float S0 = combineS0(smax, sp0, m0);
   const float ml = m0 / st;
-  const float logS0 = logf(S0);
+  const float wlo = m0 - WIN;
+  const float bHi = minp * (1.0f + 4e-6f);
+  const float bLo = minp * (1.0f - 4e-6f);
+  const float scaleM = (float)MBINS / MWIN;
+  {
+    u64t* lcand = bufA;
+    u64t* lmass = bufA + SLCAP;
+    if (deep) for (int b = tid; b < MBINS; b += TPBS) lmass[b] = 0ull;
+    __syncthreads();
+    float s0 = 0.f, sl = 0.f, sp = 0.f; int ckp = 0;
+    if (greedy) {
+      auto bodyG = [&](float vv, int gi) {
+        s0 += expf(vv - m0);
+        if (vv >= wlo) {
+          int pos = atomicAdd(&lcnt, 1);
+          if (pos < SLCAP) lcand[pos] = ((u64t)fkeyDesc(vv) << 32) | (unsigned int)gi;
+        }
+      };
+      for (int i4 = a4 + tid; i4 < b4; i4 += TPBS) {
+        float4 v = x4[i4]; int b = i4 << 2;
+        bodyG(v.x, b); bodyG(v.y, b + 1); bodyG(v.z, b + 2); bodyG(v.w, b + 3);
+      }
+      if (s == NS - 1) for (int i = (V4 << 2) + tid; i < V; i += TPBS) bodyG(x[i], i);
+    } else {
+      auto body = [&](float vv, int gi) {
+        s0 += expf(vv - m0);
+        float l = vv / st;
+        float e = expf(l - ml);
+        sl += e;
+        if (minp <= 0.f || e > bHi) {
+          sp += e; ckp++;
+          if (deep) {
+            float fm = (m0 - vv) * scaleM;
+            if (fm < (float)MBINS)
+              atomicAdd(&lmass[(int)fm], (u64t)((double)e * 4294967296.0));
+          }
+        } else if (e >= bLo) {
+          int pos = atomicAdd(&bandcnt[row], 1);
+          if (pos < BANDCAP)
+            band[(size_t)row * BANDCAP + pos] = ((u64t)(unsigned int)gi << 32) | __float_as_uint(vv);
+        }
+        if (vv >= wlo) {
+          int pos = atomicAdd(&lcnt, 1);
+          if (pos < SLCAP) lcand[pos] = ((u64t)fkeyDesc(vv) << 32) | (unsigned int)gi;
+        }
+      };
+      for (int i4 = a4 + tid; i4 < b4; i4 += TPBS) {
+        float4 v = x4[i4]; int b = i4 << 2;
+        body(v.x, b); body(v.y, b + 1); body(v.z, b + 2); body(v.w, b + 3);
+      }
+      if (s == NS - 1) for (int i = (V4 << 2) + tid; i < V; i += TPBS) body(x[i], i);
+    }
+    float r0 = blockSumF(s0, sredF);
+    float rl = blockSumF(sl, sredF);
+    float rp = blockSumF(sp, sredF);
+    int rc = blockSumI(ckp, sredI);
+    if (tid == 0) {
+      s0_ws[row * NS + s] = r0; sl_ws[row * NS + s] = rl;
+      sp_ws[row * NS + s] = rp; ck_ws[row * NS + s] = rc;
+      int c = lcnt;
+      int add = (c > SLCAP) ? (c + CAP + 1) : c;
+      lbase = atomicAdd(&ccnt[row], add);
+    }
+    __syncthreads();
+    int c = lcnt < SLCAP ? lcnt : SLCAP;
+    int base = lbase;
+    for (int j = tid; j < c; j += TPBS) {
+      int pos = base + j;
+      if (pos < CAP) cand[(size_t)row * CAP + pos] = lcand[j];
+    }
+    if (deep) {
+      u64t* mrow = mass + ((size_t)row * NS + s) * MBINS;
+      for (int b = tid; b < MBINS; b += TPBS) mrow[b] = lmass[b];
+    }
+  }
+  rowBarrier(&myBar[1]);
+
+  if (s == 0) {
+    if (tid < NS) {
+      s0s[tid] = s0_ws[row * NS + tid];
+      sls[tid] = sl_ws[row * NS + tid];
+      sps[tid] = sp_ws[row * NS + tid];
+      scks[tid] = ck_ws[row * NS + tid];
+    }
+    __syncthreads();
+    float S0 = s0s[0], S = sls[0], Sp = sps[0];
+    int ck = scks[0];
+    for (int w = 1; w < NS; ++w) { S0 += s0s[w]; S += sls[w]; Sp += sps[w]; ck += scks[w]; }
+    const float logS0 = logf(S0);
+    const float rhs = minp * (1.0f / S);
+    const float rhsS = rhs * S;
+    const float rhsHi = rhsS * (1.0f + 1e-6f);
+    const float rhsLo = rhsS * (1.0f - 1e-6f);
+    auto keepTest = [&](float e) -> bool {
+      if (e > rhsHi) return true;
+      if (e < rhsLo) return false;
+      return (e / S) >= rhs;
+    };
+
+    const int bandTotal = greedy ? 0 : bandcnt[row];
+    const bool bandOv = bandTotal > BANDCAP;
+    if (tid == 0) { sh_bCnt = 0; sh_spAdd = 0.f; sh_ckAdd = 0; }
+    __syncthreads();
+    if (!greedy && !bandOv && bandTotal > 0 && minp > 0.f) {
+      if (tid == 0) {
+        for (int i = 0; i < bandTotal; ++i) sh_bKeys[i] = band[(size_t)row * BANDCAP + i];
+        for (int i = 1; i < bandTotal; ++i) {
+          u64t k = sh_bKeys[i]; int j = i - 1;
+          while (j >= 0 && sh_bKeys[j] > k) { sh_bKeys[j + 1] = sh_bKeys[j]; j--; }
+          sh_bKeys[j + 1] = k;
+        }
+        float spAdd = 0.f; int ckAdd = 0, bc = 0;
+        for (int i = 0; i < bandTotal; ++i) {
+          float vv = __uint_as_float((unsigned int)(sh_bKeys[i] & 0xffffffffu));
+          float l = vv / st; float e = expf(l - ml);
+          if ((e / S) >= rhs) {
+            spAdd += e; ckAdd++;
+            if (deep) {
+              float fm = (m0 - vv) * scaleM;
+              if (fm < (float)MBINS) { sh_bBin[bc] = (int)fm; sh_bMass[bc] = (u64t)((double)e * 4294967296.0); bc++; }
+            }
+          }
+        }
+        sh_spAdd = spAdd; sh_ckAdd = ckAdd; sh_bCnt = bc;
+      }
+      __syncthreads();
+      Sp += sh_spAdd; ck += sh_ckAdd;
+    } else if (!greedy && bandOv) {
+      float sp2 = 0.f; int ck2 = 0;
+      auto bodyR = [&](float vv) {
+        float l = vv / st; float e = expf(l - ml);
+        if (keepTest(e)) { sp2 += e; ck2++; }
+      };
+      for (int i4 = tid; i4 < V4; i4 += TPBS) { float4 v = x4[i4]; bodyR(v.x); bodyR(v.y); bodyR(v.z); bodyR(v.w); }
+      for (int i = (V4 << 2) + tid; i < V; i += TPBS) bodyR(x[i]);
+      Sp = blockSumF(sp2, sredF);
+      ck = blockSumI(ck2, sredI);
+    }
+
+    int cc = ccnt[row];
+    int Cact = cc < CAP ? cc : CAP;
+    int need = NSEL;
+    if (topk > need) need = topk;
+    if (need > CAP / 2) need = CAP / 2;
+    if (need > V) need = V;
+    bool fb = (cc > CAP) || (Cact < need);
+    if (!fb) {
+      for (int j = tid; j < Cact; j += TPBS) bufA[j] = cand[(size_t)row * CAP + j];
+    } else {
+      int* fh = (int*)kbuf;
+      const float bS = (float)FBBINS / MWIN;
+      for (int b = tid; b < FBBINS; b += TPBS) fh[b] = 0;
+      if (tid == 0) sh_cnt = 0;
+      __syncthreads();
+      auto hb = [&](float vv) {
+        float fbv = (m0 - vv) * bS;
+        if (fbv < (float)FBBINS) atomicAdd(&fh[(int)fbv], 1);
+      };
+      for (int i4 = tid; i4 < V4; i4 += TPBS) { float4 v = x4[i4]; hb(v.x); hb(v.y); hb(v.z); hb(v.w); }
+      for (int i = (V4 << 2) + tid; i < V; i += TPBS) hb(x[i]);
+      __syncthreads();
+      int B = FBBINS - 1;
+      if (tid == 0) {
+        int cum = 0;
+        for (int b = 0; b < FBBINS; ++b) { cum += fh[b]; if (cum >= need) { B = b; break; } }
+        sredI[0] = B;
+      }
+      __syncthreads();
+      B = sredI[0];
+      __syncthreads();
+      auto cb = [&](float vv, int gi) {
+        float fbv = (m0 - vv) * bS;
+        if (fbv < (float)FBBINS && (int)fbv <= B) {
+          int pos = atomicAdd(&sh_cnt, 1);
+          if (pos < CAP) bufA[pos] = ((u64t)fkeyDesc(vv) << 32) | (unsigned int)gi;
+        }
+      };
+      for (int i4 = tid; i4 < V4; i4 += TPBS) { float4 v = x4[i4]; int b = i4 << 2; cb(v.x, b); cb(v.y, b + 1); cb(v.z, b + 2); cb(v.w, b + 3); }
+      for (int i = (V4 << 2) + tid; i < V; i += TPBS) cb(x[i], i);
+      __syncthreads();
+      Cact = sh_cnt < CAP ? sh_cnt : CAP;
+    }
+    __syncthreads();
+    {
+      int n = 128; while (n < Cact) n <<= 1;
+      for (int i = Cact + tid; i < n; i += TPBS) bufA[i] = ~0ull;
+      __syncthreads();
+      bitonicSortN(bufA, n);
+    }
+    {
+      u64t* kb64 = kbuf;
+      u64t* kbs = kbuf + NSEL;
+      int M = Cact < NSEL ? Cact : NSEL;
+      if (tid < M) {
+        u64t ka = bufA[tid];
+        float xv = fkeyInv((unsigned int)(ka >> 32));
+        float lp = (xv - m0) - logS0;
+        kb64[tid] = ((u64t)fkeyDesc(lp) << 32) | (ka & 0xffffffffu);
+      }
+      __syncthreads();
+      if (tid < M) {
+        u64t me = kb64[tid];
+        int r = 0;
+        for (int i = 0; i < M; ++i) r += (kb64[i] < me) ? 1 : 0;
+        kbs[r] = me;
+      }
+      __syncthreads();
+      float* o_idx  = out + T;
+      float* o_lps  = out + T + (size_t)T * (NL + 1);
+      for (int j = tid; j < NL; j += TPBS) {
+        if (j < M) {
+          u64t kb = kbs[j];
+          o_idx[(size_t)row * (NL + 1) + 1 + j] = (float)(unsigned int)(kb & 0xffffffffu);
+          o_lps[(size_t)row * (NL + 1) + 1 + j] = fkeyInv((unsigned int)(kb >> 32));
+        }
+      }
+    }
+
+    if (!deep) {
+      int sampled;
+      if (greedy) {
+        sampled = gidx;
+      } else {
+        if (tid == 0) {
+          int k = topk; if (k > V) k = V; if (k > CAP) k = CAP;
+          int jp = 0; float cum = 0.f;
+          for (int j = 0; j < k; ++j) {
+            float pj = 0.f;
+            if (j < ck && j < Cact) {
+              float xv = fkeyInv((unsigned int)(bufA[j] >> 32));
+              pj = expf(xv / st - ml) / Sp;
+            }
+            cum += pj;
+            float ex = cum - pj;
+            if (ex < topp) jp = j;
+          }
+          float thr;
+          if (jp < ck && jp < Cact) {
+            float xv = fkeyInv((unsigned int)(bufA[jp] >> 32));
+            thr = xv / st;
+          } else thr = -INFINITY;
+          sh_thresh = thr;
+        }
+        __syncthreads();
+        const float thr = sh_thresh;
+        float bm = -INFINITY; int bi = 0x7fffffff;
+        for (int j = tid; j < Cact; j += TPBS) {
+          u64t ka = bufA[j];
+          float xv = fkeyInv((unsigned int)(ka >> 32));
+          int gi = (int)(ka & 0xffffffffu);
+          float l = xv / st;
+          float e = expf(l - ml);
+          if (keepTest(e) && l >= thr) {
+            float uv = uu[gi];
+            float g = -logf(-logf(uv));
+            float val = l + g;
+            if (val > bm || (val == bm && gi < bi)) { bm = val; bi = gi; }
+          }
+        }
+        blockArgMaxF(bm, bi, sredF, sredI);
+        sampled = bi;
+      }
+      if (tid == 0) sh_thresh = (x[sampled] - m0) - logS0;
+      __syncthreads();
+      const float toklp = sh_thresh;
+      int rc = 0;
+      for (int j = tid; j < Cact; j += TPBS) {
+        float xv = fkeyInv((unsigned int)(bufA[j] >> 32));
+        float lp = (xv - m0) - logS0;
+        if (lp >= toklp) rc++;
+      }
+      int rank = blockSumI(rc, sredI);
+      float* o_samp = out;
+      float* o_idx  = out + T;
+      float* o_lps  = out + T + (size_t)T * (NL + 1);
+      float* o_rank = out + T + (size_t)2 * T * (NL + 1);
+      if (tid == 0) {
+        o_samp[row] = (float)sampled;
+        o_idx[(size_t)row * (NL + 1)] = (float)sampled;
+        o_lps[(size_t)row * (NL + 1)] = toklp;
+        o_rank[row] = (float)rank;
+      }
+    } else {
+      if (!bandOv) {
+        for (int b = tid; b < MBINS; b += TPBS) {
+          u64t m = 0;
+          for (int w = 0; w < NS; ++w) m += mass[((size_t)row * NS + w) * MBINS + b];
+          int bc = sh_bCnt;
+          for (int j = 0; j < bc; ++j) if (sh_bBin[j] == b) m += sh_bMass[j];
+          bufA[b] = m;
+        }
+      } else {
+        for (int b = tid; b < MBINS; b += TPBS) bufA[b] = 0ull;
+        __syncthreads();
+        auto bodyM = [&](float vv) {
+          float l = vv / st; float e = expf(l - ml);
+          if (keepTest(e)) {
+            float fm = (m0 - vv) * scaleM;
+            if (fm < (float)MBINS) atomicAdd(&bufA[(int)fm], (u64t)((double)e * 4294967296.0));
+          }
+        };
+        for (int i4 = tid; i4 < V4; i4 += TPBS) { float4 v = x4[i4]; bodyM(v.x); bodyM(v.y); bodyM(v.z); bodyM(v.w); }
+        for (int i = (V4 << 2) + tid; i < V; i += TPBS) bodyM(x[i]);
+      }
+      __syncthreads();
+      u64t v0 = bufA[tid * 4], v1 = bufA[tid * 4 + 1], v2 = bufA[tid * 4 + 2], v3 = bufA[tid * 4 + 3];
+      u64t c1 = v0 + v1, c2 = c1 + v2, tsum = c2 + v3;
+      u64t* scan = bufA + MBINS;
+      scan[tid] = tsum;
+      __syncthreads();
+      for (int off2 = 1; off2 < TPBS; off2 <<= 1) {
+        u64t add = (tid >= off2) ? scan[tid - off2] : 0ull;
+        __syncthreads();
+        scan[tid] += add;
+        __syncthreads();
+      }
+      u64t basex = scan[tid] - tsum;
+      const double TP = (double)topp * (double)Sp;
+      u64t ex0 = basex, ex1 = basex + v0, ex2 = basex + c1, ex3 = basex + c2;
+      int q = -1;
+      if (v0 > 0ull && (double)ex0 * (1.0 / 4294967296.0) < TP) q = tid * 4;
+      if (v1 > 0ull && (double)ex1 * (1.0 / 4294967296.0) < TP) q = tid * 4 + 1;
+      if (v2 > 0ull && (double)ex2 * (1.0 / 4294967296.0) < TP) q = tid * 4 + 2;
+      if (v3 > 0ull && (double)ex3 * (1.0 / 4294967296.0) < TP) q = tid * 4 + 3;
+      q = blockMaxI(q, sredI);
+      if (q >= 0 && (q >> 2) == tid) {
+        u64t e = (q & 3) == 0 ? ex0 : ((q & 3) == 1 ? ex1 : ((q & 3) == 2 ? ex2 : ex3));
+        sh_seedD = (double)e * (1.0 / 4294967296.0);
+      }
+      if (q < 0 && tid == 0) sh_seedD = 0.0;
+      __syncthreads();
+      if (tid == 0) {
+        w_bp[row] = q;
+        if (q < 0) w_thr[row] = -INFINITY;
+      }
+    }
+  }
+  if (!deep) return;
+
+  if (tid < NS) { sls[tid] = sl_ws[row * NS + tid]; s0s[tid] = s0_ws[row * NS + tid]; sps[tid] = sp_ws[row * NS + tid]; }
+  __syncthreads();
+  float S = sls[0], S0v = s0s[0], Spv = sps[0];
+  for (int w = 1; w < NS; ++w) { S += sls[w]; S0v += s0s[w]; Spv += sps[w]; }
+  if (s == 0) { Spv += sh_spAdd; }
+  const float logS0v = logf(S0v);
   const float rhs = minp * (1.0f / S);
   const float rhsS = rhs * S;
   const float rhsHi = rhsS * (1.0f + 1e-6f);
   const float rhsLo = rhsS * (1.0f - 1e-6f);
-  auto keepTest = [&](float e) -> bool {
+  auto keepTest2 = [&](float e) -> bool {
     if (e > rhsHi) return true;
     if (e < rhsLo) return false;
     return (e / S) >= rhs;
   };
-  const bool deep = (!greedy && topk <= 0);
-  const float scaleM = (float)MBINS / MWIN;
-
-  const int bandTotal = greedy ? 0 : bandcnt[row];
-  const bool bandOv = bandTotal > BANDCAP;
-  if (tid == 0) { sh_bCnt = 0; sh_spAdd = 0.f; sh_ckAdd = 0; }
-  __syncthreads();
-  if (!greedy && !bandOv && bandTotal > 0 && minp > 0.f) {
+  rowBarrier(&myBar[2]);
+  const int bp = w_bp[row];
+  if (tid == 0) lcnt = 0;
+  __syncthreads();
+  if (bp >= 0) {
+    u64t* lcand = bufA;
+    auto bodyC = [&](float vv, int gi) {
+      float fm = (m0 - vv) * scaleM;
+      if (fm < (float)MBINS && (int)fm == bp) {
+        float l = vv / st;
+        float e = expf(l - ml);
+        if (keepTest2(e)) {
+          int pos = atomicAdd(&lcnt, 1);
+          if (pos < SLCAP) lcand[pos] = ((u64t)fkeyDesc(vv) << 32) | (unsigned int)gi;
+        }
+      }
+    };
+    for (int i4 = a4 + tid; i4 < b4; i4 += TPBS) {
+      float4 v = x4[i4]; int b = i4 << 2;
+      bodyC(v.x, b); bodyC(v.y, b + 1); bodyC(v.z, b + 2); bodyC(v.w, b + 3);
+    }
+    if (s == NS - 1) for (int i = (V4 << 2) + tid; i < V; i += TPBS) bodyC(x[i], i);
+    __syncthreads();
     if (tid == 0) {
-      for (int i = 0; i < bandTotal; ++i) sh_bKeys[i] = band[(size_t)row * BANDCAP + i];
-      for (int i = 1; i < bandTotal; ++i) {
-        u64t k = sh_bKeys[i]; int j = i - 1;
-        while (j >= 0 && sh_bKeys[j] > k) { sh_bKeys[j + 1] = sh_bKeys[j]; j--; }
-        sh_bKeys[j + 1] = k;
-      }
-      float spAdd = 0.f; int ckAdd = 0, bc = 0;
-      for (int i = 0; i < bandTotal; ++i) {
-        float vv = __uint_as_float((unsigned int)(sh_bKeys[i] & 0xffffffffu));
-        float l = vv / st; float e = expf(l - ml);
-        if ((e / S) >= rhs) {
-          spAdd += e; ckAdd++;
-          if (deep) {
-            float fm = (m0 - vv) * scaleM;
-            if (fm < (float)MBINS) { sh_bBin[bc] = (int)fm; sh_bMass[bc] = (u64t)((double)e * 4294967296.0); bc++; }
-          }
-        }
-      }
-      sh_spAdd = spAdd; sh_ckAdd = ckAdd; sh_bCnt = bc;
-    }
-    __syncthreads();
-    Sp += sh_spAdd; ck += sh_ckAdd;
-  } else if (!greedy && bandOv) {
-    float sp2 = 0.f; int ck2 = 0;
-    auto bodyR = [&](float vv) {
-      float l = vv / st; float e = expf(l - ml);
-      if (keepTest(e)) { sp2 += e; ck2++; }
-    };
-    for (int i4 = tid; i4 < V4; i4 += TPB) { float4 v = x4[i4]; bodyR(v.x); bodyR(v.y); bodyR(v.z); bodyR(v.w); }
-    for (int i = (V4 << 2) + tid; i < V; i += TPB) bodyR(x[i]);
-    Sp = blockSumF(sp2, sredF);
-    ck = blockSumI(ck2, sredI);
-  }
-
-  int cc = ccnt[row];
-  int Cact = cc < CAP ? cc : CAP;
-  int need = NSEL;
-  if (topk > need) need = topk;
-  if (need > CAP / 2) need = CAP / 2;
-  if (need > V) need = V;
-  bool fb = (cc > CAP) || (Cact < need);
-  if (!fb) {
-    for (int j = tid; j < Cact; j += TPB) keyA[j] = cand[(size_t)row * CAP + j];
-  } else {
-    const float bS = (float)NBINS / MWIN;
-    for (int b = tid; b < NBINS; b += TPB) fh[b] = 0;
-    if (tid == 0) sh_cnt = 0;
-    __syncthreads();
-    auto hb = [&](float vv) {
-      float fbv = (m0 - vv) * bS;
-      if (fbv < (float)NBINS) atomicAdd(&fh[(int)fbv], 1);
-    };
-    for (int i4 = tid; i4 < V4; i4 += TPB) { float4 v = x4[i4]; hb(v.x); hb(v.y); hb(v.z); hb(v.w); }
-    for (int i = (V4 << 2) + tid; i < V; i += TPB) hb(x[i]);
-    __syncthreads();
-    if (tid == 0) {
-      int cum = 0, B = -1;
-      for (int b = 0; b < NBINS; ++b) { cum += fh[b]; if (cum >= need) { B = b; break; } }
-      if (B < 0) B = NBINS - 1;
-      sh_bp = B;
-    }
-    __syncthreads();
-    const int B = sh_bp;
-    auto cb = [&](float vv, int gi) {
-      float fbv = (m0 - vv) * bS;
-      if (fbv < (float)NBINS && (int)fbv <= B) {
-        int pos = atomicAdd(&sh_cnt, 1);
-        if (pos < CAP) keyA[pos] = ((u64t)fkeyDesc(vv) << 32) | (unsigned int)gi;
-      }
-    };
-    for (int i4 = tid; i4 < V4; i4 += TPB) { float4 v = x4[i4]; int b = i4 << 2; cb(v.x, b); cb(v.y, b + 1); cb(v.z, b + 2); cb(v.w, b + 3); }
-    for (int i = (V4 << 2) + tid; i < V; i += TPB) cb(x[i], i);
-    __syncthreads();
-    Cact = sh_cnt < CAP ? sh_cnt : CAP;
-  }
-  __syncthreads();
-  if (Cact <= 1024) {
-    u64t ka = (tid < Cact) ? keyA[tid] : ~0ull;
-    bitonicReg1024(ka, keyA);
-  } else {
-    int n = 128; while (n < Cact) n <<= 1;
-    for (int i = Cact + tid; i < n; i += TPB) keyA[i] = ~0ull;
-    __syncthreads();
-    bitonicSortN(keyA, n);
-  }
+      int c = lcnt < SLCAP ? lcnt : SLCAP;
+      lbase = atomicAdd(&ccnt2[row], c);
+    }
+    __syncthreads();
+    int c = lcnt < SLCAP ? lcnt : SLCAP;
+    int base = lbase;
+    for (int j = tid; j < c; j += TPBS) {
+      int pos = base + j;
+      if (pos < CAP) cand[(size_t)row * CAP + pos] = bufA[j];
+    }
+  }
+  rowBarrier(&myBar[3]);
+  if (s == 0 && bp >= 0) {
+    int cc2 = ccnt2[row];
+    int C5 = cc2 < CAP ? cc2 : CAP;
+    for (int j = tid; j < C5; j += TPBS) bufA[j] = cand[(size_t)row * CAP + j];
+    int n5 = 128; while (n5 < C5) n5 <<= 1;
+    for (int i = C5 + tid; i < n5; i += TPBS) bufA[i] = ~0ull;
+    __syncthreads();
+    bitonicSortN(bufA, n5);
+    if (C5 <= 1024) {
+      float* pvals = (float*)(bufA + 1024);
+      for (int j = tid; j < C5; j += TPBS) {
+        float xv = fkeyInv((unsigned int)(bufA[j] >> 32));
+        pvals[j] = expf(xv / st - ml) / Spv;
+      }
+      __syncthreads();
+      if (tid == 0) {
+        float cum = (float)(sh_seedD / (double)Spv);
+        float lastVal = fkeyInv((unsigned int)(bufA[0] >> 32));
+        for (int j = 0; j < C5; ++j) {
+          float pj = pvals[j];
+          cum += pj;
+          float ex = cum - pj;
+          if (ex < topp) lastVal = fkeyInv((unsigned int)(bufA[j] >> 32));
+        }
+        w_thr[row] = lastVal / st;
+      }
+    } else {
+      if (tid == 0) {
+        float cum = (float)(sh_seedD / (double)Spv);
+        float lastVal = fkeyInv((unsigned int)(bufA[0] >> 32));
+        for (int j = 0; j < C5; ++j) {
+          float xv = fkeyInv((unsigned int)(bufA[j] >> 32));
+          float pj = expf(xv / st - ml) / Spv;
+          cum += pj;
+          float ex = cum - pj;
+          if (ex < topp) lastVal = xv;
+        }
+        w_thr[row] = lastVal / st;
+      }
+    }
+  }
+  rowBarrier(&myBar[4]);
   {
-    int M = Cact < NSEL ? Cact : NSEL;
-    if (tid < M) {
-      u64t ka = keyA[tid];
-      float xv = fkeyInv((unsigned int)(ka >> 32));
-      float lp = (xv - m0) - logS0;
-      kb64[tid] = ((u64t)fkeyDesc(lp) << 32) | (ka & 0xffffffffu);
-    }
-    __syncthreads();
-    if (tid < M) {
-      u64t me = kb64[tid];
-      int r = 0;
-      for (int i = 0; i < M; ++i) r += (kb64[i] < me) ? 1 : 0;
-      kbs[r] = me;
-    }
-    __syncthreads();
-    float* o_idx  = out + T;
-    float* o_lps  = out + T + (size_t)T * (NL + 1);
-    for (int j = tid; j < NL; j += TPB) {
-      if (j < M) {
-        u64t kb = kbs[j];
-        o_idx[(size_t)row * (NL + 1) + 1 + j] = (float)(unsigned int)(kb & 0xffffffffu);
-        o_lps[(size_t)row * (NL + 1) + 1 + j] = fkeyInv((unsigned int)(kb >> 32));
-      }
-    }
-  }
-
-  int sampled = -1;
-  if (greedy) {
-    sampled = gidx;
-  } else if (topk > 0) {
-    if (tid == 0) {
-      int k = topk; if (k > V) k = V; if (k > CAP) k = CAP;
-      int jp = 0; float cum = 0.f;
-      for (int j = 0; j < k; ++j) {
-        float pj = 0.f;
-        if (j < ck && j < Cact) {
-          float xv = fkeyInv((unsigned int)(keyA[j] >> 32));
-          pj = expf(xv / st - ml) / Sp;
-        }
-        cum += pj;
-        float ex = cum - pj;
-        if (ex < topp) jp = j;
-      }
-      float thr;
-      if (jp < ck && jp < Cact) {
-        float xv = fkeyInv((unsigned int)(keyA[jp] >> 32));
-        thr = xv / st;
-      } else thr = -INFINITY;
-      sh_thresh = thr;
-    }
-    __syncthreads();
-    const float thr = sh_thresh;
+    const float thr = w_thr[row];
+    const float4* u4 = (const float4*)uu;
     float bm = -INFINITY; int bi = 0x7fffffff;
-    for (int j = tid; j < Cact; j += TPB) {
-      u64t ka = keyA[j];
-      float xv = fkeyInv((unsigned int)(ka >> 32));
-      int gi = (int)(ka & 0xffffffffu);
-      float l = xv / st;
+    auto body6 = [&](float vv, float uv, int gi) {
+      float l = vv / st;
       float e = expf(l - ml);
-      if (keepTest(e) && l >= thr) {
-        float uv = uu[gi];
+      if (keepTest2(e) && l >= thr) {
         float g = -logf(-logf(uv));
         float val = l + g;
         if (val > bm || (val == bm && gi < bi)) { bm = val; bi = gi; }
       }
-    }
+    };
+    for (int i4 = a4 + tid; i4 < b4; i4 += TPBS) {
+      float4 v = x4[i4]; float4 w = u4[i4]; int b = i4 << 2;
+      body6(v.x, w.x, b); body6(v.y, w.y, b + 1); body6(v.z, w.z, b + 2); body6(v.w, w.w, b + 3);
+    }
+    if (s == NS - 1) for (int i = (V4 << 2) + tid; i < V; i += TPBS) body6(x[i], uu[i], i);
     blockArgMaxF(bm, bi, sredF, sredI);
-    sampled = bi;
-  } else {
-    if (!bandOv) {
-      if (tid < MBINS) {
-        u64t m = 0;
-        for (int w = 0; w < NS; ++w) m += mass[((size_t)row * NS + w) * MBINS + tid];
-        int bc = sh_bCnt;
-        for (int j = 0; j < bc; ++j) if (sh_bBin[j] == tid) m += sh_bMass[j];
-        keyA[tid] = m;
-      }
-    } else {
-      for (int b = tid; b < MBINS; b += TPB) keyA[b] = 0ull;
-      __syncthreads();
-      auto bodyM = [&](float vv) {
-        float l = vv / st; float e = expf(l - ml);
-        if (keepTest(e)) {
-          float fm = (m0 - vv) * scaleM;
-          if (fm < (float)MBINS) atomicAdd(&keyA[(int)fm], (u64t)((double)e * 4294967296.0));
-        }
-      };
-      for (int i4 = tid; i4 < V4; i4 += TPB) { float4 v = x4[i4]; bodyM(v.x); bodyM(v.y); bodyM(v.z); bodyM(v.w); }
-      for (int i = (V4 << 2) + tid; i < V; i += TPB) bodyM(x[i]);
-    }
-    __syncthreads();
-    u64t mh = (tid < MBINS) ? keyA[tid] : 0ull;
-    for (int off = 1; off < MBINS; off <<= 1) {
-      u64t add = (tid < MBINS && tid >= off) ? keyA[tid - off] : 0ull;
-      __syncthreads();
-      if (tid < MBINS) keyA[tid] += add;
-      __syncthreads();
-    }
-    const double TP = (double)topp * (double)Sp;
-    int q = -1; u64t myexcl = 0;
-    if (tid < MBINS && mh > 0ull) {
-      u64t excl = keyA[tid] - mh;
-      if ((double)excl * (1.0 / 4294967296.0) < TP) { q = tid; myexcl = excl; }
-    }
-    int bp = blockMaxI(q, sredI);
-    if (bp >= 0 && tid == bp) sh_seed = (double)myexcl * (1.0 / 4294967296.0);
-    if (bp < 0 && tid == 0) sh_seed = 0.0;
-    __syncthreads();
-    if (tid == 0) {
-      w_bpM[row] = bp;
-      w_seed[row] = sh_seed;
-      w_spD[row] = Sp;
-      if (bp < 0) w_thr[row] = -INFINITY;
-    }
-  }
-
-  if (!deep) {
-    if (tid == 0) sh_toklp = (x[sampled] - m0) - logS0;
-    __syncthreads();
-    const float toklp = sh_toklp;
+    if (tid == 0) gkey[row * NS + s] = mkMaxKey(bm, bi);
+  }
+  rowBarrier(&myBar[5]);
+  if (s == 0 && tid == 0) {
+    u64t gk = gkey[row * NS + 0];
+    for (int w = 1; w < NS; ++w) { u64t t = gkey[row * NS + w]; if (t > gk) gk = t; }
+    int sampled = (int)(~(unsigned int)gk);
+    w_sampled[row] = sampled;
+    w_toklp[row] = (x[sampled] - m0) - logS0v;
+  }
+  rowBarrier(&myBar[6]);
+  {
+    const float toklp = w_toklp[row];
     int rc = 0;
-    for (int j = tid; j < Cact; j += TPB) {
-      float xv = fkeyInv((unsigned int)(keyA[j] >> 32));
-      float lp = (xv - m0) - logS0;
+    auto body7 = [&](float vv) {
+      float lp = (vv - m0) - logS0v;
       if (lp >= toklp) rc++;
-    }
-    int rank = blockSumI(rc, sredI);
+    };
+    for (int i4 = a4 + tid; i4 < b4; i4 += TPBS) { float4 v = x4[i4]; body7(v.x); body7(v.y); body7(v.z); body7(v.w); }
+    if (s == NS - 1) for (int i = (V4 << 2) + tid; i < V; i += TPBS) body7(x[i]);
+    int rs = blockSumI(rc, sredI);
+    if (tid == 0) atomicAdd(&rankAcc[row], rs);
+  }
+  rowBarrier(&myBar[7]);
+  if (s == 0 && tid == 0) {
+    int sampled = w_sampled[row];
     float* o_samp = out;
     float* o_idx  = out + T;
     float* o_lps  = out + T + (size_t)T * (NL + 1);
     float* o_rank = out + T + (size_t)2 * T * (NL + 1);
-    if (tid == 0) {
-      o_samp[row] = (float)sampled;
-      o_idx[(size_t)row * (NL + 1)] = (float)sampled;
-      o_lps[(size_t)row * (NL + 1)] = toklp;
-      o_rank[row] = (float)rank;
-    }
-  }
-}
-
-__global__ __launch_bounds__(TPB) void kD_thr(const float* __restrict__ logits,
-    const float* __restrict__ temp_arr, const float* __restrict__ minp_arr,
-    const float* __restrict__ topp_arr, const int* __restrict__ topk_arr,
-    const u64t* __restrict__ maxes, const float* __restrict__ sl_ws,
-    const int* __restrict__ w_bpM, const float* __restrict__ w_spD,
-    const double* __restrict__ w_seed, float* __restrict__ w_thr, int V) {
-  const int row = blockIdx.x, tid = threadIdx.x;
-  const float temp = temp_arr[row];
-  if (temp < 1e-5f || topk_arr[row] > 0) return;
-  const int bp = w_bpM[row];
-  if (bp < 0) return;
-  __shared__ u64t keyA[CAP];
-  __shared__ float pvals[CAP];
-  __shared__ u64t smax[NS];
-  __shared__ float ssl[NS];
-  __shared__ int sh_cnt;
-  if (tid < NS) { smax[tid] = maxes[row * NS + tid]; ssl[tid] = sl_ws[row * NS + tid]; }
-  if (tid == 0) sh_cnt = 0;
-  __syncthreads();
-  u64t mk = smax[0];
-  for (int w = 1; w < NS; ++w) { u64t t = smax[w]; if (t > mk) mk = t; }
-  float S = ssl[0];
-  for (int w = 1; w < NS; ++w) S += ssl[w];
-  const float m0 = ordInv((unsigned int)(mk >> 32));
-  const float st = temp;
-  const float ml = m0 / st;
-  const float minp = minp_arr[row];
-  const float rhs = minp * (1.0f / S);
-  const float rhsS = rhs * S;
-  const float rhsHi = rhsS * (1.0f + 1e-6f);
-  const float rhsLo = rhsS * (1.0f - 1e-6f);
-  auto keepTest = [&](float e) -> bool {
-    if (e > rhsHi) return true;
-    if (e < rhsLo) return false;
-    return (e / S) >= rhs;
-  };
-  const float scaleM = (float)MBINS / MWIN;
-  const float* x = logits + (size_t)row * V;
-  const int V4 = V >> 2;
-  const float4* x4 = (const float4*)x;
-  auto body = [&](float vv, int gi) {
-    float fm = (m0 - vv) * scaleM;
-    if (fm < (float)MBINS && (int)fm == bp) {
-      float l = vv / st;
-      float e = expf(l - ml);
-      if (keepTest(e)) {
-        int pos = atomicAdd(&sh_cnt, 1);
-        if (pos < CAP) keyA[pos] = ((u64t)fkeyDesc(vv) << 32) | (unsigned int)gi;
-      }
-    }
-  };
-  for (int i4 = tid; i4 < V4; i4 += TPB) {
-    float4 v = x4[i4]; int b = i4 << 2;
-    body(v.x, b); body(v.y, b + 1); body(v.z, b + 2); body(v.w, b + 3);
-  }
-  for (int i = (V4 << 2) + tid; i < V; i += TPB) body(x[i], i);
-  __syncthreads();
-  int C5 = sh_cnt < CAP ? sh_cnt : CAP;
-  if (C5 <= 1024) {
-    u64t kc = (tid < C5) ? keyA[tid] : ~0ull;
-    bitonicReg1024(kc, keyA);
-  } else {
-    int n5 = 128; while (n5 < C5) n5 <<= 1;
-    for (int i = C5 + tid; i < n5; i += TPB) keyA[i] = ~0ull;
-    __syncthreads();
-    bitonicSortN(keyA, n5);
-  }
-  const float Sp = w_spD[row];
-  for (int j = tid; j < C5; j += TPB) {
-    float xv = fkeyInv((unsigned int)(keyA[j] >> 32));
-    pvals[j] = expf(xv / st - ml) / Sp;
-  }
-  __syncthreads();
-  if (tid == 0) {
-    const float topp = topp_arr[row];
-    float cum = (float)(w_seed[row] / (double)Sp);
-    float lastVal = fkeyInv((unsigned int)(keyA[0] >> 32));
-    for (int j = 0; j < C5; ++j) {
-      float pj = pvals[j];
-      cum += pj;
-      float ex = cum - pj;
-      if (ex < topp) lastVal = fkeyInv((unsigned int)(keyA[j] >> 32));
-    }
-    w_thr[row] = lastVal / st;
-  }
-}
-
-__global__ __launch_bounds__(TPBS) void k6_gumbel(const float* __restrict__ logits,
-    const float* __restrict__ temp_arr, const float* __restrict__ minp_arr,
-    const int* __restrict__ topk_arr, const float* __restrict__ u_arr,
-    const u64t* __restrict__ maxes, const float* __restrict__ sl_ws,
-    const float* __restrict__ w_thr, u64t* __restrict__ gkey, int V) {
-  const int row = blockIdx.y, s = blockIdx.x, tid = threadIdx.x;
-  const float temp = temp_arr[row];
-  if (temp < 1e-5f || topk_arr[row] > 0) return;
-  __shared__ u64t smax[NS];
-  __shared__ float ssl[NS];
-  __shared__ float sredF[16];
-  __shared__ int sredI[16];
-  if (tid < NS) { smax[tid] = maxes[row * NS + tid]; ssl[tid] = sl_ws[row * NS + tid]; }
-  __syncthreads();
-  u64t mk = smax[0];
-  for (int w = 1; w < NS; ++w) { u64t t = smax[w]; if (t > mk) mk = t; }
-  float S = ssl[0];
-  for (int w = 1; w < NS; ++w) S += ssl[w];
-  const float m0 = ordInv((unsigned int)(mk >> 32));
-  const float st = temp;
-  const float ml = m0 / st;
-  const float minp = minp_arr[row];
-  const float rhs = minp * (1.0f / S);
-  const float rhsS = rhs * S;
-  const float rhsHi = rhsS * (1.0f + 1e-6f);
-  const float rhsLo = rhsS * (1.0f - 1e-6f);
-  auto keepTest = [&](float e) -> bool {
-    if (e > rhsHi) return true;
-    if (e < rhsLo) return false;
-    return (e / S) >= rhs;
-  };
-  const float thr = w_thr[row];
-  const float* x  = logits + (size_t)row * V;
-  const float* uu = u_arr  + (size_t)row * V;
-  const int V4 = V >> 2;
-  const float4* x4 = (const float4*)x;
-  const float4* u4 = (const float4*)uu;
-  const int a4 = (int)(((long long)V4 * s) / NS), b4 = (int)(((long long)V4 * (s + 1)) / NS);
-  float bm = -INFINITY; int bi = 0x7fffffff;
-  auto body = [&](float vv, float uv, int gi) {
-    float l = vv / st;
-    float e = expf(l - ml);
-    if (keepTest(e) && l >= thr) {
-      float g = -logf(-logf(uv));
-      float val = l + g;
-      if (val > bm || (val == bm && gi < bi)) { bm = val; bi = gi; }
-    }
-  };
-  for (int i4 = a4 + tid; i4 < b4; i4 += TPBS) {
-    float4 v = x4[i4]; float4 w = u4[i4]; int b = i4 << 2;
-    body(v.x, w.x, b); body(v.y, w.y, b + 1); body(v.z, w.z, b + 2); body(v.w, w.w, b + 3);
-  }
-  if (s == NS - 1) for (int i = (V4 << 2) + tid; i < V; i += TPBS) body(x[i], uu[i], i);
-  blockArgMaxF(bm, bi, sredF, sredI);
-  if (tid == 0) gkey[row * NS + s] = mkMaxKey(bm, bi);
-}
-
-__global__ __launch_bounds__(TPB) void k7_deepfin(const float* __restrict__ logits,
-    const float* __restrict__ temp_arr, const int* __restrict__ topk_arr,
-    const u64t* __restrict__ gkey, const float* __restrict__ s0_ws,
-    const u64t* __restrict__ maxes, float* __restrict__ out, int T, int V, int NL) {
-  const int row = blockIdx.x, tid = threadIdx.x;
-  const float temp = temp_arr[row];
-  if (temp < 1e-5f || topk_arr[row] > 0) return;
-  __shared__ u64t sg[NS];
-  __shared__ u64t smax[NS];
-  __shared__ float sp0[NS];
-  __shared__ int sredI[16];
-  if (tid < NS) { sg[tid] = gkey[row * NS + tid]; smax[tid] = maxes[row * NS + tid]; sp0[tid] = s0_ws[row * NS + tid]; }
-  __syncthreads();
-  u64t gk = sg[0];
-  for (int w = 1; w < NS; ++w) { if (sg[w] > gk) gk = sg[w]; }
-  u64t mk = smax[0];
-  for (int w = 1; w < NS; ++w) { u64t t = smax[w]; if (t > mk) mk = t; }
-  const float m0 = ordInv((unsigned int)(mk >> 32));
-  const float S0 = combineS0(smax, sp0, m0);
-  const float logS0 = logf(S0);
-  const int sampled = (int)(~(unsigned int)gk);
-  const float* x = logits + (size_t)row * V;
-  const float toklp = (x[sampled] - m0) - logS0;
-  const int V4 = V >> 2;
-  const float4* x4 = (const float4*)x;
-  int rc = 0;
-  auto body = [&](float vv) {
-    float lp = (vv - m0) - logS0;
-    if (lp >= toklp) rc++;
-  };
-  for (int i4 = tid; i4 < V4; i4 += TPB) { float4 v = x4[i4]; body(v.x); body(v.y); body(v.z); body(v.w); }
-  for (int i = (V4 << 2) + tid; i < V; i += TPB) body(x[i]);
-  int rank = blockSumI(rc, sredI);
-  float* o_samp = out;
-  float* o_idx  = out + T;
-  float* o_lps  = out + T + (size_t)T * (NL + 1);
-  float* o_rank = out + T + (size_t)2 * T * (NL + 1);
-  if (tid == 0) {
     o_samp[row] = (float)sampled;
     o_idx[(size_t)row * (NL + 1)] = (float)sampled;
-    o_lps[(size_t)row * (NL + 1)] = toklp;
-    o_rank[row] = (float)rank;
+    o_lps[(size_t)row * (NL + 1)] = w_toklp[row];
+    o_rank[row] = (float)rankAcc[row];
   }
 }
 
@@ -1187,21 +1083,27 @@
 
   size_t off = 0;
   char* base = (char*)d_ws;
-  u64t*   w_maxes   = (u64t*)(base + off);   off += (size_t)T * NS * 8;
-  u64t*   w_cand    = (u64t*)(base + off);   off += (size_t)T * CAP * 8;
-  u64t*   w_mass    = (u64t*)(base + off);   off += (size_t)T * NS * MBINS * 8;
-  u64t*   w_gkey    = (u64t*)(base + off);   off += (size_t)T * NS * 8;
-  u64t*   w_band    = (u64t*)(base + off);   off += (size_t)T * BANDCAP * 8;
-  double* w_seed    = (double*)(base + off); off += (size_t)T * 8;
-  float*  w_s0      = (float*)(base + off);  off += (size_t)T * NS * 4;
-  float*  w_sl      = (float*)(base + off);  off += (size_t)T * NS * 4;
-  float*  w_sp      = (float*)(base + off);  off += (size_t)T * NS * 4;
-  int*    w_ck      = (int*)(base + off);    off += (size_t)T * NS * 4;
-  int*    w_ccnt    = (int*)(base + off);    off += (size_t)T * 4;
-  int*    w_bandcnt = (int*)(base + off);    off += (size_t)T * 4;
-  float*  w_thr     = (float*)(base + off);  off += (size_t)T * 4;
-  int*    w_bpM     = (int*)(base + off);    off += (size_t)T * 4;
-  float*  w_spD     = (float*)(base + off);  off += (size_t)T * 4;
+  u64t* w_maxes = (u64t*)(base + off); off += (size_t)T * NS * 8;
+  u64t* w_cand  = (u64t*)(base + off); off += (size_t)T * CAP * 8;
+  u64t* w_mass  = (u64t*)(base + off); off += (size_t)T * NS * MBINS * 8;
+  u64t* w_gkey  = (u64t*)(base + off); off += (size_t)T * NS * 8;
+  u64t* w_band  = (u64t*)(base + off); off += (size_t)T * BANDCAP * 8;
+  float* w_s0   = (float*)(base + off); off += (size_t)T * NS * 4;
+  float* w_sl   = (float*)(base + off); off += (size_t)T * NS * 4;
+  float* w_sp   = (float*)(base + off); off += (size_t)T * NS * 4;
+  int*   w_ck   = (int*)(base + off);   off += (size_t)T * NS * 4;
+  float* w_thr  = (float*)(base + off); off += (size_t)T * 4;
+  int*   w_bp   = (int*)(base + off);   off += (size_t)T * 4;
+  int*   w_samp = (int*)(base + off);   off += (size_t)T * 4;
+  float* w_tlp  = (float*)(base + off); off += (size_t)T * 4;
+  int* w_zero = (int*)(base + off);
+  int nZero = T * (NBAR + 4);
+  off += (size_t)nZero * 4;
+  int* w_bars    = w_zero;
+  int* w_ccnt    = w_zero + T * NBAR;
+  int* w_bandcnt = w_ccnt + T;
+  int* w_ccnt2   = w_bandcnt + T;
+  int* w_rankAcc = w_ccnt2 + T;
 
   if (off > ws_size) {
     sampler_mono<<<T, TPB, 0, stream>>>(logits, temp, minp, topp, topk, u,
@@ -1209,19 +1111,11 @@
     return;
   }
 
-  dim3 gS(NS, T);
-  k1_max<<<gS, TPBS, 0, stream>>>(logits, w_maxes, w_s0, w_ccnt, w_bandcnt, V);
-  k2_all<<<gS, TPBS, 0, stream>>>(logits, temp, minp, topk, w_maxes, w_sl,
-                                  w_sp, w_ck, w_ccnt, w_cand, w_bandcnt, w_band,
-                                  w_mass, V);
-  k5_final<<<T, TPB, 0, stream>>>(logits, temp, minp, topp, topk, u, w_maxes,
-                                  w_s0, w_sl, w_sp, w_ck, w_ccnt, w_cand, w_mass,
-                                  w_band, w_bandcnt, w_thr, w_bpM, w_seed, w_spD,
-                                  (float*)d_out, T, V, NL);
-  kD_thr<<<T, TPB, 0, stream>>>(logits, temp, minp, topp, topk, w_maxes, w_sl,
-                                w_bpM, w_spD, w_seed, w_thr, V);
-  k6_gumbel<<<gS, TPBS, 0, stream>>>(logits, temp, minp, topk, u, w_maxes, w_sl,
-                                     w_thr, w_gkey, V);
-  k7_deepfin<<<T, TPB, 0, stream>>>(logits, temp, topk, w_gkey, w_s0, w_maxes,
-                                    (float*)d_out, T, V, NL);
-}
+  k0_zero<<<(nZero + 255) / 256, 256, 0, stream>>>(w_zero, nZero);
+  dim3 g(NS, T);
+  fused<<<g, TPBS, 0, stream>>>(logits, temp, minp, topp, topk, u,
+                                w_maxes, w_cand, w_mass, w_gkey, w_band,
+                                w_s0, w_sl, w_sp, w_ck, w_ccnt, w_bandcnt,
+                                w_ccnt2, w_rankAcc, w_thr, w_bp, w_samp, w_tlp,
+                                w_bars, (float*)d_out, T, V, NL);
+}
```

After: 655.0 us. 3.08x slower.
